# Kernel optimization log

Hardware: AMD Instinct MI355X
Metric: run time of the kernel (lower is better)

## Reference

```python
import math
import jax, jax.numpy as jnp
import numpy as np

N, E, EA = 25000, 400000, 400000
DN, DE, H = 256, 128, 8
DHN, DHE = DN // H, DE // H
EPS = 1e-5


def _ln(x, g, b):
    m = x.mean(-1, keepdims=True)
    v = ((x - m) ** 2).mean(-1, keepdims=True)
    return (x - m) * jax.lax.rsqrt(v + EPS) * g + b


def _scatter_softmax(scores, index, n):
    # per-segment stable softmax (matches torch scatter_reduce amax + scatter_add)
    m = jnp.maximum(jax.ops.segment_max(scores, index, num_segments=n), -1e9)
    ex = jnp.exp(scores - m[index])
    den = jax.ops.segment_sum(ex, index, num_segments=n)
    return ex / (den[index] + 1e-10)


def setup_inputs() -> dict:
    key = jax.random.key(0)
    ks = iter(jax.random.split(key, 64))
    rn = lambda shape, s=0.02: jax.random.normal(next(ks), shape, jnp.float32) * s
    inp = {
        'node_features': jax.random.normal(next(ks), (N, DN), jnp.float32),
        'edge_features': jax.random.normal(next(ks), (E, DE), jnp.float32),
        'edge_index': jax.random.randint(next(ks), (2, E), 0, N),
        'edge_adj': jax.random.randint(next(ks), (2, EA), 0, E),
        # NodeAttention params
        'n_Wq': rn((DN, DN)), 'n_bq': jnp.zeros(DN), 'n_Wk': rn((DN, DN)), 'n_bk': jnp.zeros(DN),
        'n_Wv': rn((DN, DN)), 'n_bv': jnp.zeros(DN), 'n_Web': rn((DE, H)), 'n_beb': jnp.zeros(H),
        'n_Wo': rn((DN, DN)), 'n_bo': jnp.zeros(DN), 'n_logt': jnp.zeros(H),
        'n_g': jnp.ones(DN), 'n_b': jnp.zeros(DN),
        # EdgeAttention params
        'e_Wq': rn((DE, DE)), 'e_bq': jnp.zeros(DE), 'e_Wk': rn((DE, DE)), 'e_bk': jnp.zeros(DE),
        'e_Wv': rn((DE, DE)), 'e_bv': jnp.zeros(DE), 'e_Wctx': rn((2 * DN, H)), 'e_bctx': jnp.zeros(H),
        'e_Wo': rn((DE, DE)), 'e_bo': jnp.zeros(DE), 'e_logt': jnp.zeros(H),
        'e_g': jnp.ones(DE), 'e_b': jnp.zeros(DE),
        # ReconciliationBridge params
        'r_We': rn((DE + 2 * DN, DE)), 'r_be': jnp.zeros(DE), 'r_eg': jnp.ones(DE), 'r_ebt': jnp.zeros(DE),
        'r_Wn': rn((DN + DE, DN)), 'r_bn': jnp.zeros(DN), 'r_ng': jnp.ones(DN), 'r_nbt': jnp.zeros(DN),
    }
    return inp


def reference(node_features, edge_features, edge_index, edge_adj,
              n_Wq, n_bq, n_Wk, n_bk, n_Wv, n_bv, n_Web, n_beb, n_Wo, n_bo, n_logt, n_g, n_b,
              e_Wq, e_bq, e_Wk, e_bk, e_Wv, e_bv, e_Wctx, e_bctx, e_Wo, e_bo, e_logt, e_g, e_b,
              r_We, r_be, r_eg, r_ebt, r_Wn, r_bn, r_ng, r_nbt):
    Nn, En = node_features.shape[0], edge_features.shape[0]
    src, tgt = edge_index[0], edge_index[1]

    # ---- NodeAttention (uses original node/edge features) ----
    x = node_features
    Q = (x @ n_Wq + n_bq).reshape(Nn, H, DHN)
    K = (x @ n_Wk + n_bk).reshape(Nn, H, DHN)
    V = (x @ n_Wv + n_bv).reshape(Nn, H, DHN)
    s = (Q[tgt] * K[src]).sum(-1) / math.sqrt(DHN)            # [E, H]
    s = (s + edge_features @ n_Web + n_beb) * jnp.exp(n_logt)
    w = _scatter_softmax(s, tgt, Nn)
    agg = jax.ops.segment_sum(V[src] * w[..., None], tgt, num_segments=Nn).reshape(Nn, DN)
    node_out = _ln(x + agg @ n_Wo + n_bo, n_g, n_b)

    # ---- EdgeAttention (uses original node/edge features) ----
    e = edge_features
    Qe = (e @ e_Wq + e_bq).reshape(En, H, DHE)
    Ke = (e @ e_Wk + e_bk).reshape(En, H, DHE)
    Ve = (e @ e_Wv + e_bv).reshape(En, H, DHE)
    se, te = edge_adj[0], edge_adj[1]
    s2 = (Qe[te] * Ke[se]).sum(-1) / math.sqrt(DHE)           # [EA, H]
    ctx = jnp.concatenate([node_features[src[se]], node_features[tgt[se]]], -1)
    s2 = (s2 + ctx @ e_Wctx + e_bctx) * jnp.exp(e_logt)
    w2 = _scatter_softmax(s2, te, En)
    agg2 = jax.ops.segment_sum(Ve[se] * w2[..., None], te, num_segments=En).reshape(En, DE)
    edge_out = _ln(e + agg2 @ e_Wo + e_bo, e_g, e_b)

    # ---- ReconciliationBridge on updated features ----
    edge_ctx = jnp.concatenate([edge_out, node_out[src], node_out[tgt]], -1)
    new_edges = _ln(edge_out + edge_ctx @ r_We + r_be, r_eg, r_ebt)
    all_nodes = jnp.concatenate([src, tgt])
    all_edges = jnp.concatenate([new_edges, new_edges], 0)
    esum = jax.ops.segment_sum(all_edges, all_nodes, num_segments=Nn)
    ecnt = jax.ops.segment_sum(jnp.ones(all_nodes.shape[0], jnp.float32), all_nodes, num_segments=Nn)
    emean = esum / (ecnt[:, None] + 1e-10)
    node_ctx = jnp.concatenate([node_out, emean], -1)
    new_nodes = _ln(node_out + node_ctx @ r_Wn + r_bn, r_ng, r_nbt)
    return new_nodes, new_edges
```

## Files before the change

kernel.cpp:

```cpp
#include <hip/hip_runtime.h>
#include <cstdio>
#include <cstddef>

typedef unsigned short u16;
typedef unsigned int u32;

#define DEVFN __device__ __forceinline__

namespace {
constexpr int NN = 25000;
constexpr int NE = 400000;
constexpr int NA = 400000;
constexpr int DN = 256;
constexpr int DE = 128;
constexpr int H  = 8;
constexpr float LN_EPS = 1e-5f;
}

DEVFN float bf2f(u32 x) { union { u32 u; float f; } v; v.u = x << 16; return v.f; }
DEVFN u16 f2bf(float f) {
    u32 u = __float_as_uint(f);
    u32 r = 0x7fffu + ((u >> 16) & 1u);
    return (u16)((u + r) >> 16);
}
DEVFN void unpack8(uint4 v, float* f) {
    f[0] = bf2f(v.x & 0xffffu); f[1] = bf2f(v.x >> 16);
    f[2] = bf2f(v.y & 0xffffu); f[3] = bf2f(v.y >> 16);
    f[4] = bf2f(v.z & 0xffffu); f[5] = bf2f(v.z >> 16);
    f[6] = bf2f(v.w & 0xffffu); f[7] = bf2f(v.w >> 16);
}

typedef __bf16 bf16x8 __attribute__((ext_vector_type(8)));
typedef float f32x4 __attribute__((ext_vector_type(4)));
union B8 { uint4 u; bf16x8 b; };

template<int B> struct IO;
template<> struct IO<1> {
    static DEVFN float ld(const void* p, size_t i) { return bf2f(((const u16*)p)[i]); }
    static DEVFN void ld8(const void* p, size_t i, float* f) {
        unpack8(*reinterpret_cast<const uint4*>((const u16*)p + i), f);
    }
    static DEVFN void st(void* p, size_t i, float v) { ((u16*)p)[i] = f2bf(v); }
};
template<> struct IO<0> {
    static DEVFN float ld(const void* p, size_t i) { return ((const float*)p)[i]; }
    static DEVFN void ld8(const void* p, size_t i, float* f) {
        const float* q = (const float*)p + i;
        float4 a = *reinterpret_cast<const float4*>(q);
        float4 b = *reinterpret_cast<const float4*>(q + 4);
        f[0]=a.x; f[1]=a.y; f[2]=a.z; f[3]=a.w; f[4]=b.x; f[5]=b.y; f[6]=b.z; f[7]=b.w;
    }
    static DEVFN void st(void* p, size_t i, float v) { ((float*)p)[i] = v; }
};

__global__ void k_detect(const void* ng, int* flag) {
    if (threadIdx.x == 0 && blockIdx.x == 0) {
        const u16* p = (const u16*)ng;
        int zeros = 0;
        for (int i = 0; i < 64; i += 2) if (p[i] == 0) ++zeros;
        *flag = (zeros >= 16) ? 0 : 1;
    }
}

__global__ __launch_bounds__(256) void k_fill(float* p, long n, float v) {
    long i = (long)blockIdx.x * 256 + threadIdx.x;
    long st = (long)gridDim.x * 256;
    for (; i < n; i += st) p[i] = v;
}

__global__ __launch_bounds__(256) void k_transpose(
    const int* dflag, const u16* __restrict__ in, u16* __restrict__ out, int K, int Nd)
{
    if (*dflag != 1) return;
    int gid = blockIdx.x * 256 + threadIdx.x;
    if (gid >= K * Nd) return;
    int n = gid / K, k = gid - n * K;
    out[gid] = in[(size_t)k * Nd + n];
}

__global__ __launch_bounds__(256) void k_gemm_mfma(
    const int* dflag, const u16* __restrict__ A, const u16* __restrict__ Wt,
    const u16* __restrict__ bias, u16* __restrict__ out, int M, int K, int Nd)
{
    if (*dflag != 1) return;
    __shared__ __align__(16) char shbuf[128 * 128];
    const int t = threadIdx.x;
    const int m0 = blockIdx.x * 64;
    const int n0 = blockIdx.y * 128;
    const int w = t >> 6;
    const int lane = t & 63;
    const int lm = lane & 15, lg = lane >> 4;
    const int NC = K >> 6;

    uint4 sreg[4];
    auto gstage = [&](int kc) {
#pragma unroll
        for (int it = 0; it < 4; ++it) {
            int idx = it * 256 + t;
            int n = idx >> 3, slot = idx & 7;
            sreg[it] = *reinterpret_cast<const uint4*>(Wt + (size_t)(n0 + n) * K + kc * 64 + slot * 8);
        }
    };
    auto swrite = [&]() {
#pragma unroll
        for (int it = 0; it < 4; ++it) {
            int idx = it * 256 + t;
            int n = idx >> 3, slot = idx & 7;
            *reinterpret_cast<uint4*>(shbuf + n * 128 + ((slot ^ (n & 7)) * 16)) = sreg[it];
        }
    };

    f32x4 acc[4][2];
    const f32x4 z = {0.f, 0.f, 0.f, 0.f};
#pragma unroll
    for (int mf = 0; mf < 4; ++mf)
#pragma unroll
        for (int nf = 0; nf < 2; ++nf) acc[mf][nf] = z;

    gstage(0); swrite();
    for (int kc = 0; kc < NC; ++kc) {
        if (kc + 1 < NC) gstage(kc + 1);
        __syncthreads();
#pragma unroll
        for (int ksl = 0; ksl < 2; ++ksl) {
            B8 a[4];
#pragma unroll
            for (int mf = 0; mf < 4; ++mf) {
                int r = m0 + mf * 16 + lm;
                if (r >= M) r = M - 1;
                a[mf].u = *reinterpret_cast<const uint4*>(A + (size_t)r * K + kc * 64 + ksl * 32 + lg * 8);
            }
#pragma unroll
            for (int nf = 0; nf < 2; ++nf) {
                int n = w * 32 + nf * 16 + lm;
                int slot = ksl * 4 + lg;
                B8 bfrag;
                bfrag.u = *reinterpret_cast<const uint4*>(shbuf + n * 128 + ((slot ^ (n & 7)) * 16));
#pragma unroll
                for (int mf = 0; mf < 4; ++mf)
                    acc[mf][nf] = __builtin_amdgcn_mfma_f32_16x16x32_bf16(a[mf].b, bfrag.b, acc[mf][nf], 0, 0, 0);
            }
        }
        __syncthreads();
        if (kc + 1 < NC) swrite();
    }
#pragma unroll
    for (int mf = 0; mf < 4; ++mf)
#pragma unroll
        for (int nf = 0; nf < 2; ++nf) {
            int col = n0 + w * 32 + nf * 16 + lm;
            float bb = bf2f(bias[col]);
#pragma unroll
            for (int j = 0; j < 4; ++j) {
                int gr = m0 + mf * 16 + lg * 4 + j;
                if (gr < M) out[(size_t)gr * Nd + col] = f2bf(acc[mf][nf][j] + bb);
            }
        }
}

template<int B>
__global__ __launch_bounds__(256) void k_edge_bias(
    const int* dflag, const void* __restrict__ ef, const void* __restrict__ Web,
    const void* __restrict__ beb, float* __restrict__ s)
{
    if (*dflag != B) return;
    __shared__ float Wsh[DE * H];
    __shared__ float bsh[H];
    for (int i = threadIdx.x; i < DE * H; i += 256) Wsh[i] = IO<B>::ld(Web, i);
    if (threadIdx.x < H) bsh[threadIdx.x] = IO<B>::ld(beb, threadIdx.x);
    __syncthreads();
    int gid = blockIdx.x * 256 + threadIdx.x;
    if (gid >= NE * H) return;
    int e = gid >> 3, h = gid & 7;
    float acc = 0.f;
    for (int k = 0; k < DE; k += 8) {
        float a[8]; IO<B>::ld8(ef, (size_t)e * DE + k, a);
#pragma unroll
        for (int j = 0; j < 8; ++j) acc += a[j] * Wsh[(k + j) * H + h];
    }
    s[gid] = acc + bsh[h];
}

template<int B>
__global__ __launch_bounds__(256) void k_ctx_bias(
    const int* dflag, const void* __restrict__ nf,
    const int* __restrict__ src, const int* __restrict__ tgt,
    const void* __restrict__ Wctx, const void* __restrict__ bctx, float* __restrict__ ebias)
{
    if (*dflag != B) return;
    __shared__ float Wsh[2 * DN * H];
    __shared__ float bsh[H];
    for (int i = threadIdx.x; i < 2 * DN * H; i += 256) Wsh[i] = IO<B>::ld(Wctx, i);
    if (threadIdx.x < H) bsh[threadIdx.x] = IO<B>::ld(bctx, threadIdx.x);
    __syncthreads();
    int gid = blockIdx.x * 256 + threadIdx.x;
    if (gid >= NE * H) return;
    int e = gid >> 3, h = gid & 7;
    int is = src[e], it = tgt[e];
    if ((unsigned)is >= NN || (unsigned)it >= NN) { ebias[gid] = 0.f; return; }
    float acc = 0.f;
    for (int k = 0; k < DN; k += 8) {
        float a[8]; IO<B>::ld8(nf, (size_t)is * DN + k, a);
#pragma unroll
        for (int j = 0; j < 8; ++j) acc += a[j] * Wsh[(k + j) * H + h];
    }
    for (int k = 0; k < DN; k += 8) {
        float a[8]; IO<B>::ld8(nf, (size_t)it * DN + k, a);
#pragma unroll
        for (int j = 0; j < 8; ++j) acc += a[j] * Wsh[(DN + k + j) * H + h];
    }
    ebias[gid] = acc + bsh[h];
}

template<int B>
__global__ __launch_bounds__(256) void k_node_score(
    const int* dflag, const u16* __restrict__ Q, const u16* __restrict__ Kt,
    const int* __restrict__ src, const int* __restrict__ tgt,
    const void* __restrict__ logt, float* __restrict__ s, float* __restrict__ den)
{
    if (*dflag != B) return;
    int gid = blockIdx.x * 256 + threadIdx.x;
    if (gid >= NE * H) return;
    int e = gid >> 3, h = gid & 7;
    int te = tgt[e], se = src[e];
    if ((unsigned)te >= NN || (unsigned)se >= NN) { s[gid] = 0.f; return; }
    const u16* q = Q + (size_t)te * DN + h * 32;
    const u16* k = Kt + (size_t)se * DN + h * 32;
    float acc = 0.f;
#pragma unroll
    for (int i = 0; i < 4; ++i) {
        float qa[8], ka[8];
        unpack8(*reinterpret_cast<const uint4*>(q + i * 8), qa);
        unpack8(*reinterpret_cast<const uint4*>(k + i * 8), ka);
#pragma unroll
        for (int j = 0; j < 8; ++j) acc += qa[j] * ka[j];
    }
    float val = (acc * 0.17677669529663689f + s[gid]) * expf(IO<B>::ld(logt, h));
    float ex = expf(fminf(val, 60.f));
    s[gid] = ex;
    atomicAdd(&den[(size_t)te * H + h], ex);
}

__global__ __launch_bounds__(256) void k_node_agg(
    const u16* __restrict__ V, const int* __restrict__ src, const int* __restrict__ tgt,
    const float* __restrict__ s, const float* __restrict__ den, float* __restrict__ agg)
{
    long gid = (long)blockIdx.x * 256 + threadIdx.x;
    if (gid >= (long)NE * DN) return;
    int e = (int)(gid >> 8);
    int c = (int)(gid & 255);
    int h = c >> 5;
    int te = tgt[e], se = src[e];
    if ((unsigned)te >= NN || (unsigned)se >= NN) return;
    float w = s[(size_t)e * H + h] / (den[(size_t)te * H + h] + 1e-10f);
    float v = bf2f(V[(size_t)se * DN + c]);
    atomicAdd(&agg[(size_t)te * DN + c], v * w);
}

template<int B>
__global__ __launch_bounds__(256) void k_edge_score(
    const int* dflag, const u16* __restrict__ Qe, const u16* __restrict__ Ke,
    const int* __restrict__ se, const int* __restrict__ te,
    const void* __restrict__ logt, const float* __restrict__ ebias,
    float* __restrict__ s2, float* __restrict__ den2)
{
    if (*dflag != B) return;
    int gid = blockIdx.x * 256 + threadIdx.x;
    if (gid >= NA * H) return;
    int a = gid >> 3, h = gid & 7;
    int tE = te[a], sE = se[a];
    if ((unsigned)tE >= NE || (unsigned)sE >= NE) { s2[gid] = 0.f; return; }
    const u16* q = Qe + (size_t)tE * DE + h * 16;
    const u16* k = Ke + (size_t)sE * DE + h * 16;
    float acc = 0.f;
#pragma unroll
    for (int i = 0; i < 2; ++i) {
        float qa[8], ka[8];
        unpack8(*reinterpret_cast<const uint4*>(q + i * 8), qa);
        unpack8(*reinterpret_cast<const uint4*>(k + i * 8), ka);
#pragma unroll
        for (int j = 0; j < 8; ++j) acc += qa[j] * ka[j];
    }
    float val = (acc * 0.25f + ebias[(size_t)sE * H + h]) * expf(IO<B>::ld(logt, h));
    float ex = expf(fminf(val, 60.f));
    s2[gid] = ex;
    atomicAdd(&den2[(size_t)tE * H + h], ex);
}

__global__ __launch_bounds__(256) void k_edge_agg(
    const u16* __restrict__ Ve, const int* __restrict__ se, const int* __restrict__ te,
    const float* __restrict__ s2, const float* __restrict__ den2, float* __restrict__ agg2)
{
    long gid = (long)blockIdx.x * 256 + threadIdx.x;
    if (gid >= (long)NA * DE) return;
    int a = (int)(gid >> 7);
    int c = (int)(gid & 127);
    int h = c >> 4;
    int tE = te[a], sE = se[a];
    if ((unsigned)tE >= NE || (unsigned)sE >= NE) return;
    float w = s2[(size_t)a * H + h] / (den2[(size_t)tE * H + h] + 1e-10f);
    float v = bf2f(Ve[(size_t)sE * DE + c]);
    atomicAdd(&agg2[(size_t)tE * DE + c], v * w);
}

template<int B>
__global__ __launch_bounds__(256) void k_node_out(
    const int* dflag, const float* __restrict__ agg, const void* __restrict__ x,
    const void* __restrict__ Wo, const void* __restrict__ bo,
    const void* __restrict__ g, const void* __restrict__ b, u16* __restrict__ nout)
{
    if (*dflag != B) return;
    __shared__ __align__(16) float As[32][36];
    __shared__ __align__(16) float Ws[32][264];
    const int t = threadIdx.x;
    const int m0 = blockIdx.x * 32;
    const int r0 = (t >> 5) * 4;
    const int c0 = (t & 31) * 8;
    const int arow = t >> 3, akk = (t & 7) * 4;
    const int wrow = t >> 3, wcc = (t & 7) * 32;
    float acc[4][8] = {};
    for (int k0 = 0; k0 < DN; k0 += 32) {
        float av[4];
        const int gr = m0 + arow;
        if (gr < NN) {
            float4 v = *reinterpret_cast<const float4*>(agg + (size_t)gr * DN + k0 + akk);
            av[0] = v.x; av[1] = v.y; av[2] = v.z; av[3] = v.w;
        } else { av[0] = av[1] = av[2] = av[3] = 0.f; }
        float wv[32];
#pragma unroll
        for (int u = 0; u < 4; ++u)
            IO<B>::ld8(Wo, (size_t)(k0 + wrow) * DN + wcc + u * 8, wv + u * 8);
        __syncthreads();
#pragma unroll
        for (int j = 0; j < 4; ++j) As[akk + j][arow] = av[j];
#pragma unroll
        for (int j = 0; j < 32; ++j) Ws[wrow][wcc + j] = wv[j];
        __syncthreads();
#pragma unroll
        for (int kk = 0; kk < 32; ++kk) {
            float4 a4 = *reinterpret_cast<const float4*>(&As[kk][r0]);
            float4 wa = *reinterpret_cast<const float4*>(&Ws[kk][c0]);
            float4 wb = *reinterpret_cast<const float4*>(&Ws[kk][c0 + 4]);
            float aa[4] = {a4.x, a4.y, a4.z, a4.w};
            float ww[8] = {wa.x, wa.y, wa.z, wa.w, wb.x, wb.y, wb.z, wb.w};
#pragma unroll
            for (int i = 0; i < 4; ++i)
#pragma unroll
                for (int j = 0; j < 8; ++j) acc[i][j] += aa[i] * ww[j];
        }
        __syncthreads();
    }
    float gv[8], bv[8], bov[8];
#pragma unroll
    for (int j = 0; j < 8; ++j) {
        gv[j] = IO<B>::ld(g, c0 + j); bv[j] = IO<B>::ld(b, c0 + j); bov[j] = IO<B>::ld(bo, c0 + j);
    }
#pragma unroll
    for (int i = 0; i < 4; ++i) {
        int gr = m0 + r0 + i;
        if (gr >= NN) continue;
        float xv[8]; IO<B>::ld8(x, (size_t)gr * DN + c0, xv);
        float val[8]; float sum = 0.f, sq = 0.f;
#pragma unroll
        for (int j = 0; j < 8; ++j) {
            val[j] = acc[i][j] + xv[j] + bov[j];
            sum += val[j]; sq += val[j] * val[j];
        }
#pragma unroll
        for (int msk = 1; msk < 32; msk <<= 1) {
            sum += __shfl_xor(sum, msk, 64);
            sq += __shfl_xor(sq, msk, 64);
        }
        float mu = sum * (1.f / DN);
        float var = fmaxf(sq * (1.f / DN) - mu * mu, 0.f);
        float rstd = rsqrtf(var + LN_EPS);
        u16* o = nout + (size_t)gr * DN + c0;
#pragma unroll
        for (int j = 0; j < 8; ++j) o[j] = f2bf((val[j] - mu) * rstd * gv[j] + bv[j]);
    }
}

template<int B>
__global__ __launch_bounds__(256) void k_edge_out(
    const int* dflag, const float* __restrict__ agg2, const void* __restrict__ ef,
    const void* __restrict__ Wo, const void* __restrict__ bo,
    const void* __restrict__ g, const void* __restrict__ b, u16* __restrict__ eout)
{
    if (*dflag != B) return;
    __shared__ __align__(16) float As[32][68];
    __shared__ __align__(16) float Ws[32][136];
    const int t = threadIdx.x;
    const int m0 = blockIdx.x * 64;
    const int r0 = (t >> 4) * 4;
    const int c0 = (t & 15) * 8;
    const int arow = t >> 2, akk = (t & 3) * 8;
    const int wrow = t >> 3, wcc = (t & 7) * 16;
    float acc[4][8] = {};
    for (int k0 = 0; k0 < DE; k0 += 32) {
        float av[8];
        {
            const float* p = agg2 + (size_t)(m0 + arow) * DE + k0 + akk;
            float4 v0 = *reinterpret_cast<const float4*>(p);
            float4 v1 = *reinterpret_cast<const float4*>(p + 4);
            av[0] = v0.x; av[1] = v0.y; av[2] = v0.z; av[3] = v0.w;
            av[4] = v1.x; av[5] = v1.y; av[6] = v1.z; av[7] = v1.w;
        }
        float wv[16];
        IO<B>::ld8(Wo, (size_t)(k0 + wrow) * DE + wcc, wv);
        IO<B>::ld8(Wo, (size_t)(k0 + wrow) * DE + wcc + 8, wv + 8);
        __syncthreads();
#pragma unroll
        for (int j = 0; j < 8; ++j) As[akk + j][arow] = av[j];
#pragma unroll
        for (int j = 0; j < 16; ++j) Ws[wrow][wcc + j] = wv[j];
        __syncthreads();
#pragma unroll
        for (int kk = 0; kk < 32; ++kk) {
            float4 a4 = *reinterpret_cast<const float4*>(&As[kk][r0]);
            float4 wa = *reinterpret_cast<const float4*>(&Ws[kk][c0]);
            float4 wb = *reinterpret_cast<const float4*>(&Ws[kk][c0 + 4]);
            float aa[4] = {a4.x, a4.y, a4.z, a4.w};
            float ww[8] = {wa.x, wa.y, wa.z, wa.w, wb.x, wb.y, wb.z, wb.w};
#pragma unroll
            for (int i = 0; i < 4; ++i)
#pragma unroll
                for (int j = 0; j < 8; ++j) acc[i][j] += aa[i] * ww[j];
        }
        __syncthreads();
    }
    float gv[8], bv[8], bov[8];
#pragma unroll
    for (int j = 0; j < 8; ++j) {
        gv[j] = IO<B>::ld(g, c0 + j); bv[j] = IO<B>::ld(b, c0 + j); bov[j] = IO<B>::ld(bo, c0 + j);
    }
#pragma unroll
    for (int i = 0; i < 4; ++i) {
        int gr = m0 + r0 + i;
        float xv[8]; IO<B>::ld8(ef, (size_t)gr * DE + c0, xv);
        float val[8]; float sum = 0.f, sq = 0.f;
#pragma unroll
        for (int j = 0; j < 8; ++j) {
            val[j] = acc[i][j] + xv[j] + bov[j];
            sum += val[j]; sq += val[j] * val[j];
        }
#pragma unroll
        for (int msk = 1; msk < 16; msk <<= 1) {
            sum += __shfl_xor(sum, msk, 64);
            sq += __shfl_xor(sq, msk, 64);
        }
        float mu = sum * (1.f / DE);
        float var = fmaxf(sq * (1.f / DE) - mu * mu, 0.f);
        float rstd = rsqrtf(var + LN_EPS);
        u16* o = eout + (size_t)gr * DE + c0;
#pragma unroll
        for (int j = 0; j < 8; ++j) o[j] = f2bf((val[j] - mu) * rstd * gv[j] + bv[j]);
    }
}

__global__ __launch_bounds__(256) void k_bridge_edge_mfma(
    const int* dflag, const u16* __restrict__ eout, const u16* __restrict__ nout,
    const int* __restrict__ src, const int* __restrict__ tgt,
    const u16* __restrict__ Wt, const u16* __restrict__ be,
    const u16* __restrict__ g, const u16* __restrict__ b,
    u16* __restrict__ out_edges)
{
    if (*dflag != 1) return;
    __shared__ __align__(16) char shbuf[64 * 132 * 4];
    __shared__ int es_sh[64], et_sh[64];
    const int t = threadIdx.x;
    const int m0 = blockIdx.x * 64;
    if (t < 64) {
        int a = src[m0 + t], c = tgt[m0 + t];
        es_sh[t] = ((unsigned)a < NN) ? a : 0;
        et_sh[t] = ((unsigned)c < NN) ? c : 0;
    }
    const int w = t >> 6;
    const int lane = t & 63;
    const int lm = lane & 15, lg = lane >> 4;
    constexpr int K = 640, NC = 10;

    uint4 sreg[4];
    auto gstage = [&](int kc) {
#pragma unroll
        for (int it = 0; it < 4; ++it) {
            int idx = it * 256 + t;
            int n = idx >> 3, slot = idx & 7;
            sreg[it] = *reinterpret_cast<const uint4*>(Wt + (size_t)n * K + kc * 64 + slot * 8);
        }
    };
    auto swrite = [&]() {
#pragma unroll
        for (int it = 0; it < 4; ++it) {
            int idx = it * 256 + t;
            int n = idx >> 3, slot = idx & 7;
            *reinterpret_cast<uint4*>(shbuf + n * 128 + ((slot ^ (n & 7)) * 16)) = sreg[it];
        }
    };

    f32x4 acc[4][2];
    const f32x4 z = {0.f, 0.f, 0.f, 0.f};
#pragma unroll
    for (int mf = 0; mf < 4; ++mf)
#pragma unroll
        for (int nf = 0; nf < 2; ++nf) acc[mf][nf] = z;

    gstage(0); swrite();
    for (int kc = 0; kc < NC; ++kc) {
        if (kc + 1 < NC) gstage(kc + 1);
        __syncthreads();
#pragma unroll
        for (int ksl = 0; ksl < 2; ++ksl) {
            B8 a[4];
#pragma unroll
            for (int mf = 0; mf < 4; ++mf) {
                int rloc = mf * 16 + lm;
                const u16* ap;
                if (kc < 2)      ap = eout + (size_t)(m0 + rloc) * DE + kc * 64;
                else if (kc < 6) ap = nout + (size_t)es_sh[rloc] * DN + (kc - 2) * 64;
                else             ap = nout + (size_t)et_sh[rloc] * DN + (kc - 6) * 64;
                a[mf].u = *reinterpret_cast<const uint4*>(ap + ksl * 32 + lg * 8);
            }
#pragma unroll
            for (int nf = 0; nf < 2; ++nf) {
                int n = w * 32 + nf * 16 + lm;
                int slot = ksl * 4 + lg;
                B8 bfrag;
                bfrag.u = *reinterpret_cast<const uint4*>(shbuf + n * 128 + ((slot ^ (n & 7)) * 16));
#pragma unroll
                for (int mf = 0; mf < 4; ++mf)
                    acc[mf][nf] = __builtin_amdgcn_mfma_f32_16x16x32_bf16(a[mf].b, bfrag.b, acc[mf][nf], 0, 0, 0);
            }
        }
        __syncthreads();
        if (kc + 1 < NC) swrite();
    }
    float* cex = (float*)shbuf;
#pragma unroll
    for (int mf = 0; mf < 4; ++mf)
#pragma unroll
        for (int nf = 0; nf < 2; ++nf)
#pragma unroll
            for (int j = 0; j < 4; ++j)
                cex[(mf * 16 + lg * 4 + j) * 132 + (w * 32 + nf * 16 + lm)] = acc[mf][nf][j];
    __syncthreads();
    {
        const int row = t >> 2, seg = t & 3;
        const int gr = m0 + row;
        const int cb = seg * 32;
        float v[32]; float sum = 0.f, sq = 0.f;
#pragma unroll
        for (int u = 0; u < 4; ++u) {
            float ev[8], bev[8];
            unpack8(*reinterpret_cast<const uint4*>(eout + (size_t)gr * DE + cb + u * 8), ev);
            unpack8(*reinterpret_cast<const uint4*>(be + cb + u * 8), bev);
#pragma unroll
            for (int j = 0; j < 8; ++j) {
                float x = cex[row * 132 + cb + u * 8 + j] + ev[j] + bev[j];
                v[u * 8 + j] = x; sum += x; sq += x * x;
            }
        }
        sum += __shfl_xor(sum, 1, 64); sq += __shfl_xor(sq, 1, 64);
        sum += __shfl_xor(sum, 2, 64); sq += __shfl_xor(sq, 2, 64);
        float mu = sum * (1.f / DE);
        float rstd = rsqrtf(fmaxf(sq * (1.f / DE) - mu * mu, 0.f) + LN_EPS);
#pragma unroll
        for (int u = 0; u < 4; ++u) {
            float gv[8], bv[8];
            unpack8(*reinterpret_cast<const uint4*>(g + cb + u * 8), gv);
            unpack8(*reinterpret_cast<const uint4*>(b + cb + u * 8), bv);
#pragma unroll
            for (int j = 0; j < 8; ++j)
                out_edges[(size_t)gr * DE + cb + u * 8 + j] = f2bf((v[u * 8 + j] - mu) * rstd * gv[j] + bv[j]);
        }
    }
}

template<int B>
__global__ __launch_bounds__(256) void k_gemm_bias(
    const int* dflag, const void* __restrict__ A, const void* __restrict__ W,
    const void* __restrict__ bias, u16* __restrict__ out, int M, int K, int Nd)
{
    if (*dflag != B) return;
    __shared__ __align__(16) float As[32][72];
    __shared__ __align__(16) float Ws[32][68];
    const int t = threadIdx.x;
    const int m0 = blockIdx.x * 64;
    const int n0 = blockIdx.y * 64;
    const int r0 = (t >> 4) * 4;
    const int c0 = (t & 15) * 4;
    const int arow = t >> 2, akk = (t & 3) * 8;
    const int wrow = t >> 3, wcc = (t & 7) * 8;
    float acc[4][4] = {};
    for (int k0 = 0; k0 < K; k0 += 32) {
        float av[8];
        const int gr = m0 + arow;
        if (gr < M) IO<B>::ld8(A, (size_t)gr * K + k0 + akk, av);
        else { for (int j = 0; j < 8; ++j) av[j] = 0.f; }
        float wv[8];
        IO<B>::ld8(W, (size_t)(k0 + wrow) * Nd + n0 + wcc, wv);
        __syncthreads();
#pragma unroll
        for (int j = 0; j < 8; ++j) As[akk + j][arow] = av[j];
#pragma unroll
        for (int j = 0; j < 8; ++j) Ws[wrow][wcc + j] = wv[j];
        __syncthreads();
#pragma unroll
        for (int kk = 0; kk < 32; ++kk) {
            float4 a4 = *reinterpret_cast<const float4*>(&As[kk][r0]);
            float4 w4 = *reinterpret_cast<const float4*>(&Ws[kk][c0]);
            float aa[4] = {a4.x, a4.y, a4.z, a4.w};
            float ww[4] = {w4.x, w4.y, w4.z, w4.w};
#pragma unroll
            for (int i = 0; i < 4; ++i)
#pragma unroll
                for (int j = 0; j < 4; ++j) acc[i][j] += aa[i] * ww[j];
        }
        __syncthreads();
    }
    float bv[4];
#pragma unroll
    for (int j = 0; j < 4; ++j) bv[j] = IO<B>::ld(bias, n0 + c0 + j);
#pragma unroll
    for (int i = 0; i < 4; ++i) {
        int gr = m0 + r0 + i;
        if (gr < M) {
            u16* o = out + (size_t)gr * Nd + n0 + c0;
#pragma unroll
            for (int j = 0; j < 4; ++j) o[j] = f2bf(acc[i][j] + bv[j]);
        }
    }
}

template<int B>
__global__ __launch_bounds__(256) void k_bridge_edge(
    const int* dflag, const u16* __restrict__ eout, const u16* __restrict__ nout,
    const int* __restrict__ src, const int* __restrict__ tgt,
    const void* __restrict__ We, const void* __restrict__ be,
    const void* __restrict__ g, const void* __restrict__ b,
    void* __restrict__ out_edges)
{
    if (*dflag != B) return;
    __shared__ __align__(16) float As[32][68];
    __shared__ __align__(16) float Ws[32][136];
    __shared__ int es[64], et[64];
    const int t = threadIdx.x;
    const int m0 = blockIdx.x * 64;
    if (t < 64) {
        int a = src[m0 + t], c = tgt[m0 + t];
        es[t] = ((unsigned)a < NN) ? a : 0;
        et[t] = ((unsigned)c < NN) ? c : 0;
    }
    __syncthreads();
    const int r0 = (t >> 4) * 4;
    const int c0 = (t & 15) * 8;
    const int arow = t >> 2, akk = (t & 3) * 8;
    const int wrow = t >> 3, wcc = (t & 7) * 16;
    float acc[4][8] = {};
    for (int k0 = 0; k0 < 640; k0 += 32) {
        const u16* aptr;
        if (k0 < 128)      aptr = eout + (size_t)(m0 + arow) * DE + k0 + akk;
        else if (k0 < 384) aptr = nout + (size_t)es[arow] * DN + (k0 - 128) + akk;
        else               aptr = nout + (size_t)et[arow] * DN + (k0 - 384) + akk;
        float av[8]; unpack8(*reinterpret_cast<const uint4*>(aptr), av);
        float wv[16];
        IO<B>::ld8(We, (size_t)(k0 + wrow) * DE + wcc, wv);
        IO<B>::ld8(We, (size_t)(k0 + wrow) * DE + wcc + 8, wv + 8);
        __syncthreads();
#pragma unroll
        for (int j = 0; j < 8; ++j) As[akk + j][arow] = av[j];
#pragma unroll
        for (int j = 0; j < 16; ++j) Ws[wrow][wcc + j] = wv[j];
        __syncthreads();
#pragma unroll
        for (int kk = 0; kk < 32; ++kk) {
            float4 a4 = *reinterpret_cast<const float4*>(&As[kk][r0]);
            float4 wa = *reinterpret_cast<const float4*>(&Ws[kk][c0]);
            float4 wb = *reinterpret_cast<const float4*>(&Ws[kk][c0 + 4]);
            float aa[4] = {a4.x, a4.y, a4.z, a4.w};
            float ww[8] = {wa.x, wa.y, wa.z, wa.w, wb.x, wb.y, wb.z, wb.w};
#pragma unroll
            for (int i = 0; i < 4; ++i)
#pragma unroll
                for (int j = 0; j < 8; ++j) acc[i][j] += aa[i] * ww[j];
        }
        __syncthreads();
    }
    float gv[8], bv[8], bev[8];
#pragma unroll
    for (int j = 0; j < 8; ++j) {
        gv[j] = IO<B>::ld(g, c0 + j); bv[j] = IO<B>::ld(b, c0 + j); bev[j] = IO<B>::ld(be, c0 + j);
    }
#pragma unroll
    for (int i = 0; i < 4; ++i) {
        int r = r0 + i;
        int gr = m0 + r;
        float val[8]; float sum = 0.f, sq = 0.f;
#pragma unroll
        for (int j = 0; j < 8; ++j) {
            val[j] = acc[i][j] + bf2f(eout[(size_t)gr * DE + c0 + j]) + bev[j];
            sum += val[j]; sq += val[j] * val[j];
        }
#pragma unroll
        for (int msk = 1; msk < 16; msk <<= 1) {
            sum += __shfl_xor(sum, msk, 64);
            sq += __shfl_xor(sq, msk, 64);
        }
        float mu = sum * (1.f / DE);
        float var = fmaxf(sq * (1.f / DE) - mu * mu, 0.f);
        float rstd = rsqrtf(var + LN_EPS);
#pragma unroll
        for (int j = 0; j < 8; ++j) {
            float ov = (val[j] - mu) * rstd * gv[j] + bv[j];
            IO<B>::st(out_edges, (size_t)gr * DE + c0 + j, ov);
        }
    }
}

__global__ __launch_bounds__(256) void k_deg(
    const int* __restrict__ src, const int* __restrict__ tgt, int* __restrict__ cnt)
{
    int e = blockIdx.x * 256 + threadIdx.x;
    if (e >= NE) return;
    int a = src[e]; a = ((unsigned)a < NN) ? a : 0;
    int c = tgt[e]; c = ((unsigned)c < NN) ? c : 0;
    atomicAdd(&cnt[a], 1);
    atomicAdd(&cnt[c], 1);
}

__global__ __launch_bounds__(256) void k_scan(
    const int* __restrict__ cnt, int* __restrict__ off, int* __restrict__ cur, int n)
{
    __shared__ int sh[256];
    __shared__ int carry;
    const int t = threadIdx.x;
    if (t == 0) carry = 0;
    __syncthreads();
    for (int base = 0; base < n; base += 256) {
        int i = base + t;
        int v = (i < n) ? cnt[i] : 0;
        sh[t] = v;
        __syncthreads();
#pragma unroll
        for (int d = 1; d < 256; d <<= 1) {
            int x = (t >= d) ? sh[t - d] : 0;
            __syncthreads();
            sh[t] += x;
            __syncthreads();
        }
        int incl = sh[t];
        int total = sh[255];
        if (i < n) {
            off[i + 1] = carry + incl;
            cur[i] = carry + incl - v;
        }
        __syncthreads();
        if (t == 0) carry += total;
        __syncthreads();
    }
    if (t == 0) off[0] = 0;
}

__global__ __launch_bounds__(256) void k_place(
    const int* __restrict__ src, const int* __restrict__ tgt,
    int* __restrict__ cur, int* __restrict__ ent)
{
    int e = blockIdx.x * 256 + threadIdx.x;
    if (e >= NE) return;
    int a = src[e]; a = ((unsigned)a < NN) ? a : 0;
    int c = tgt[e]; c = ((unsigned)c < NN) ? c : 0;
    int p = atomicAdd(&cur[a], 1); ent[p] = e;
    p = atomicAdd(&cur[c], 1);     ent[p] = e;
}

template<int B>
__global__ __launch_bounds__(256) void k_esum_gather(
    const int* dflag, const void* __restrict__ edges ,
    const int* __restrict__ off, const int* __restrict__ ent,
    float* __restrict__ esum, float* __restrict__ ecnt)
{
    if (*dflag != B) return;
    int node = blockIdx.x * 4 + (threadIdx.x >> 6);
    if (node >= NN) return;
    int lane = threadIdx.x & 63;
    int b0 = off[node], b1 = off[node + 1];
    float a0 = 0.f, a1 = 0.f;
    for (int i = b0; i < b1; ++i) {
        int e = ent[i];
        size_t base = (size_t)e * DE;
        a0 += IO<B>::ld(edges, base + lane);
        a1 += IO<B>::ld(edges, base + 64 + lane);
    }
    esum[(size_t)node * DE + lane] = a0;
    esum[(size_t)node * DE + 64 + lane] = a1;
    if (lane == 0) ecnt[node] = (float)(b1 - b0);
}

template<int B>
__global__ __launch_bounds__(256) void k_bridge_node(
    const int* dflag, const u16* __restrict__ nout,
    const float* __restrict__ esum, const float* __restrict__ ecnt,
    const void* __restrict__ Wn, const void* __restrict__ bn,
    const void* __restrict__ g, const void* __restrict__ b, void* __restrict__ out_nodes)
{
    if (*dflag != B) return;
    __shared__ __align__(16) float As[32][36];
    __shared__ __align__(16) float Ws[32][264];
    __shared__ float rc[32];
    const int t = threadIdx.x;
    const int m0 = blockIdx.x * 32;
    if (t < 32) {
        int gr = m0 + t;
        rc[t] = (gr < NN) ? 1.f / (ecnt[gr] + 1e-10f) : 0.f;
    }
    __syncthreads();
    const int r0 = (t >> 5) * 4;
    const int c0 = (t & 31) * 8;
    const int arow = t >> 3, akk = (t & 7) * 4;
    const int wrow = t >> 3, wcc = (t & 7) * 32;
    float acc[4][8] = {};
    for (int k0 = 0; k0 < 384; k0 += 32) {
        float av[4];
        const int gr = m0 + arow;
        if (gr < NN) {
            if (k0 < 256) {
                uint2 v = *reinterpret_cast<const uint2*>(nout + (size_t)gr * DN + k0 + akk);
                av[0] = bf2f(v.x & 0xffffu); av[1] = bf2f(v.x >> 16);
                av[2] = bf2f(v.y & 0xffffu); av[3] = bf2f(v.y >> 16);
            } else {
                float4 v = *reinterpret_cast<const float4*>(esum + (size_t)gr * DE + (k0 - 256) + akk);
                float r = rc[arow];
                av[0] = v.x * r; av[1] = v.y * r; av[2] = v.z * r; av[3] = v.w * r;
            }
        } else { av[0] = av[1] = av[2] = av[3] = 0.f; }
        float wv[32];
#pragma unroll
        for (int u = 0; u < 4; ++u)
            IO<B>::ld8(Wn, (size_t)(k0 + wrow) * DN + wcc + u * 8, wv + u * 8);
        __syncthreads();
#pragma unroll
        for (int j = 0; j < 4; ++j) As[akk + j][arow] = av[j];
#pragma unroll
        for (int j = 0; j < 32; ++j) Ws[wrow][wcc + j] = wv[j];
        __syncthreads();
#pragma unroll
        for (int kk = 0; kk < 32; ++kk) {
            float4 a4 = *reinterpret_cast<const float4*>(&As[kk][r0]);
            float4 wa = *reinterpret_cast<const float4*>(&Ws[kk][c0]);
            float4 wb = *reinterpret_cast<const float4*>(&Ws[kk][c0 + 4]);
            float aa[4] = {a4.x, a4.y, a4.z, a4.w};
            float ww[8] = {wa.x, wa.y, wa.z, wa.w, wb.x, wb.y, wb.z, wb.w};
#pragma unroll
            for (int i = 0; i < 4; ++i)
#pragma unroll
                for (int j = 0; j < 8; ++j) acc[i][j] += aa[i] * ww[j];
        }
        __syncthreads();
    }
    float gv[8], bv[8], bnv[8];
#pragma unroll
    for (int j = 0; j < 8; ++j) {
        gv[j] = IO<B>::ld(g, c0 + j); bv[j] = IO<B>::ld(b, c0 + j); bnv[j] = IO<B>::ld(bn, c0 + j);
    }
#pragma unroll
    for (int i = 0; i < 4; ++i) {
        int gr = m0 + r0 + i;
        if (gr >= NN) continue;
        float val[8]; float sum = 0.f, sq = 0.f;
#pragma unroll
        for (int j = 0; j < 8; ++j) {
            val[j] = acc[i][j] + bf2f(nout[(size_t)gr * DN + c0 + j]) + bnv[j];
            sum += val[j]; sq += val[j] * val[j];
        }
#pragma unroll
        for (int msk = 1; msk < 32; msk <<= 1) {
            sum += __shfl_xor(sum, msk, 64);
            sq += __shfl_xor(sq, msk, 64);
        }
        float mu = sum * (1.f / DN);
        float var = fmaxf(sq * (1.f / DN) - mu * mu, 0.f);
        float rstd = rsqrtf(var + LN_EPS);
#pragma unroll
        for (int j = 0; j < 8; ++j)
            IO<B>::st(out_nodes, (size_t)gr * DN + c0 + j, (val[j] - mu) * rstd * gv[j] + bv[j]);
    }
}

extern "C" void kernel_launch(void* const* d_in, const int* in_sizes, int n_in,
                              void* d_out, int out_size, void* d_ws, size_t ws_size,
                              hipStream_t stream)
{
    if (n_in < 38 || in_sizes[0] != NN * DN || in_sizes[1] != NE * DE) {
        fprintf(stderr, "kernel_launch: unexpected inputs n_in=%d sz0=%d sz1=%d\n",
                n_in, in_sizes[0], n_in > 1 ? in_sizes[1] : -1);
        return;
    }
    const void* nf  = d_in[0];
    const void* ef  = d_in[1];
    const int* eidx = (const int*)d_in[2];
    const int* eadj = (const int*)d_in[3];
    const int* srcN = eidx;
    const int* tgtN = eidx + NE;
    const int* seA  = eadj;
    const int* teA  = eadj + NA;
    const void *nWq = d_in[4],  *nbq  = d_in[5];
    const void *nWk = d_in[6],  *nbk  = d_in[7];
    const void *nWv = d_in[8],  *nbv  = d_in[9];
    const void *nWeb = d_in[10], *nbeb = d_in[11];
    const void *nWo = d_in[12], *nbo  = d_in[13];
    const void *nlogt = d_in[14], *ng = d_in[15], *nb = d_in[16];
    const void *eWq = d_in[17], *ebq  = d_in[18];
    const void *eWk = d_in[19], *ebk  = d_in[20];
    const void *eWv = d_in[21], *ebv  = d_in[22];
    const void *eWctx = d_in[23], *ebctx = d_in[24];
    const void *eWo = d_in[25], *ebo  = d_in[26];
    const void *elogt = d_in[27], *eg = d_in[28], *ebb = d_in[29];
    const void *rWe = d_in[30], *rbe  = d_in[31];
    const void *reg_ = d_in[32], *rebt = d_in[33];
    const void *rWn = d_in[34], *rbn  = d_in[35];
    const void *rng = d_in[36], *rnbt = d_in[37];

    char* ws = (char*)d_ws;
    size_t off = 0;
    auto take = [&](size_t bytes) -> char* {
        char* p = ws + off;
        off = (off + bytes + 255) & ~(size_t)255;
        return p;
    };
    int*   flag     = (int*)  take(256);
    u16*   node_out = (u16*)  take((size_t)NN * DN * 2);
    u16*   edge_out = (u16*)  take((size_t)NE * DE * 2);
    float* esum     = (float*)take((size_t)NN * DE * 4);
    float* ecnt     = (float*)take((size_t)NN * 4);
    u16* WtQn = (u16*)take((size_t)DN * DN * 2);
    u16* WtKn = (u16*)take((size_t)DN * DN * 2);
    u16* WtVn = (u16*)take((size_t)DN * DN * 2);
    u16* WtQe = (u16*)take((size_t)DE * DE * 2);
    u16* WtKe = (u16*)take((size_t)DE * DE * 2);
    u16* WtVe = (u16*)take((size_t)DE * DE * 2);
    u16* WtWe = (u16*)take((size_t)640 * DE * 2);
    const size_t T = off;
    u16*   Qn   = (u16*)(ws + T);
    u16*   Kn   = Qn + (size_t)NN * DN;
    u16*   Vn   = Kn + (size_t)NN * DN;
    float* sA   = (float*)(Vn + (size_t)NN * DN);
    float* denA = sA + (size_t)NE * H;
    float* aggA = denA + (size_t)NN * H;
    size_t endA = (size_t)((char*)(aggA + (size_t)NN * DN) - ws);
    u16*   Qe    = (u16*)(ws + T);
    u16*   Ke    = Qe + (size_t)NE * DE;
    float* agg2  = (float*)Ke;
    float* ebias = (float*)(ws + T + (size_t)NE * DE * 2 + (size_t)NE * DE * 4);
    float* s2    = ebias + (size_t)NE * H;
    float* den2  = s2 + (size_t)NA * H;
    size_t endB = (size_t)((char*)(den2 + (size_t)NE * H) - ws);
    int* c_off = (int*)(ws + T);
    int* c_cur = c_off + (NN + 1);
    int* c_ent = c_cur + NN;
    size_t endC = (size_t)((char*)(c_ent + (size_t)2 * NE) - ws);
    size_t need = endA > endB ? endA : endB;
    if (endC > need) need = endC;
    if (ws_size < need) {
        fprintf(stderr, "kernel_launch: ws_size=%zu < needed=%zu\n", ws_size, need);
        return;
    }

    auto fill = [&](float* p, long n, float v) {
        long blocks = (n + 255) / 256;
        if (blocks > 8192) blocks = 8192;
        k_fill<<<dim3((unsigned)blocks), dim3(256), 0, stream>>>(p, n, v);
    };

    k_detect<<<1, 64, 0, stream>>>(ng, flag);

    auto T2D = [&](const void* W, u16* Wt, int K, int Nd) {
        k_transpose<<<dim3((unsigned)((K * Nd + 255) / 256)), 256, 0, stream>>>(flag, (const u16*)W, Wt, K, Nd);
    };
    T2D(nWq, WtQn, DN, DN); T2D(nWk, WtKn, DN, DN); T2D(nWv, WtVn, DN, DN);
    T2D(eWq, WtQe, DE, DE); T2D(eWk, WtKe, DE, DE); T2D(eWv, WtVe, DE, DE);
    T2D(rWe, WtWe, 640, DE);

    fill(denA, (long)NN * H, 0.f);
    fill(aggA, (long)NN * DN, 0.f);
    dim3 gA((NN + 63) / 64, DN / 64);
    dim3 gAm((NN + 63) / 64, DN / 128);
    k_gemm_mfma<<<gAm, 256, 0, stream>>>(flag, (const u16*)nf, WtQn, (const u16*)nbq, Qn, NN, DN, DN);
    k_gemm_bias<0><<<gA, 256, 0, stream>>>(flag, nf, nWq, nbq, Qn, NN, DN, DN);
    k_gemm_mfma<<<gAm, 256, 0, stream>>>(flag, (const u16*)nf, WtKn, (const u16*)nbk, Kn, NN, DN, DN);
    k_gemm_bias<0><<<gA, 256, 0, stream>>>(flag, nf, nWk, nbk, Kn, NN, DN, DN);
    k_gemm_mfma<<<gAm, 256, 0, stream>>>(flag, (const u16*)nf, WtVn, (const u16*)nbv, Vn, NN, DN, DN);
    k_gemm_bias<0><<<gA, 256, 0, stream>>>(flag, nf, nWv, nbv, Vn, NN, DN, DN);
    const int gEH = (NE * H + 255) / 256;
    k_edge_bias<1><<<gEH, 256, 0, stream>>>(flag, ef, nWeb, nbeb, sA);
    k_edge_bias<0><<<gEH, 256, 0, stream>>>(flag, ef, nWeb, nbeb, sA);
    k_node_score<1><<<gEH, 256, 0, stream>>>(flag, Qn, Kn, srcN, tgtN, nlogt, sA, denA);
    k_node_score<0><<<gEH, 256, 0, stream>>>(flag, Qn, Kn, srcN, tgtN, nlogt, sA, denA);
    {
        long n = (long)NE * DN;
        k_node_agg<<<dim3((unsigned)((n + 255) / 256)), 256, 0, stream>>>(Vn, srcN, tgtN, sA, denA, aggA);
    }
    k_node_out<1><<<(NN + 31) / 32, 256, 0, stream>>>(flag, aggA, nf, nWo, nbo, ng, nb, node_out);
    k_node_out<0><<<(NN + 31) / 32, 256, 0, stream>>>(flag, aggA, nf, nWo, nbo, ng, nb, node_out);

    dim3 gB(NE / 64, DE / 64);
    dim3 gBm(NE / 64, DE / 128);
    k_gemm_mfma<<<gBm, 256, 0, stream>>>(flag, (const u16*)ef, WtQe, (const u16*)ebq, Qe, NE, DE, DE);
    k_gemm_bias<0><<<gB, 256, 0, stream>>>(flag, ef, eWq, ebq, Qe, NE, DE, DE);
    k_gemm_mfma<<<gBm, 256, 0, stream>>>(flag, (const u16*)ef, WtKe, (const u16*)ebk, Ke, NE, DE, DE);
    k_gemm_bias<0><<<gB, 256, 0, stream>>>(flag, ef, eWk, ebk, Ke, NE, DE, DE);
    k_ctx_bias<1><<<gEH, 256, 0, stream>>>(flag, nf, srcN, tgtN, eWctx, ebctx, ebias);
    k_ctx_bias<0><<<gEH, 256, 0, stream>>>(flag, nf, srcN, tgtN, eWctx, ebctx, ebias);
    fill(den2, (long)NE * H, 0.f);
    const int gAH = (NA * H + 255) / 256;
    k_edge_score<1><<<gAH, 256, 0, stream>>>(flag, Qe, Ke, seA, teA, elogt, ebias, s2, den2);
    k_edge_score<0><<<gAH, 256, 0, stream>>>(flag, Qe, Ke, seA, teA, elogt, ebias, s2, den2);
    k_gemm_mfma<<<gBm, 256, 0, stream>>>(flag, (const u16*)ef, WtVe, (const u16*)ebv, Qe , NE, DE, DE);
    k_gemm_bias<0><<<gB, 256, 0, stream>>>(flag, ef, eWv, ebv, Qe , NE, DE, DE);
    fill(agg2, (long)NE * DE, 0.f);
    {
        long n = (long)NA * DE;
        k_edge_agg<<<dim3((unsigned)((n + 255) / 256)), 256, 0, stream>>>(Qe , seA, teA, s2, den2, agg2);
    }
    k_edge_out<1><<<NE / 64, 256, 0, stream>>>(flag, agg2, ef, eWo, ebo, eg, ebb, edge_out);
    k_edge_out<0><<<NE / 64, 256, 0, stream>>>(flag, agg2, ef, eWo, ebo, eg, ebb, edge_out);

    void* out_nodes = d_out;
    void* out_edges_bf = (void*)((u16*)d_out + (size_t)NN * DN);
    void* out_edges_f  = (void*)((float*)d_out + (size_t)NN * DN);
    k_bridge_edge_mfma<<<NE / 64, 256, 0, stream>>>(flag, edge_out, node_out, srcN, tgtN,
                                                    WtWe, (const u16*)rbe, (const u16*)reg_, (const u16*)rebt,
                                                    (u16*)out_edges_bf);
    k_bridge_edge<0><<<NE / 64, 256, 0, stream>>>(flag, edge_out, node_out, srcN, tgtN,
                                                  rWe, rbe, reg_, rebt, out_edges_f);
    fill((float*)c_cur, NN, 0.f);
    k_deg<<<(NE + 255) / 256, 256, 0, stream>>>(srcN, tgtN, c_cur);
    k_scan<<<1, 256, 0, stream>>>(c_cur , c_off, c_cur , NN);
    k_place<<<(NE + 255) / 256, 256, 0, stream>>>(srcN, tgtN, c_cur, c_ent);
    k_esum_gather<1><<<(NN + 3) / 4, 256, 0, stream>>>(flag, out_edges_bf, c_off, c_ent, esum, ecnt);
    k_esum_gather<0><<<(NN + 3) / 4, 256, 0, stream>>>(flag, out_edges_f, c_off, c_ent, esum, ecnt);
    k_bridge_node<1><<<(NN + 31) / 32, 256, 0, stream>>>(flag, node_out, esum, ecnt,
                                                         rWn, rbn, rng, rnbt, out_nodes);
    k_bridge_node<0><<<(NN + 31) / 32, 256, 0, stream>>>(flag, node_out, esum, ecnt,
                                                         rWn, rbn, rng, rnbt, out_nodes);
}
```

Measured before the change: 3.770 ms.

## Move output projections and bridge node GEMM to MFMA, unify fp32/bf16 paths

Replaces the scalar FP32 shared-memory GEMMs in node_out, edge_out and bridge_node with bf16 MFMA tiles. Their weights are pre-transposed and converted once per call, and the accumulators are staged through LDS for the fused residual+LayerNorm epilogue. The MFMA GEMM is templated so the fp32 input path also uses MFMA by packing activations to bf16 on load. This cuts FP32 ALU time on the dense projections, at the cost of bf16 rounding of agg and activations and extra transpose launches.

```diff
diff --git a/kernel.cpp b/kernel.cpp
--- a/kernel.cpp
+++ b/kernel.cpp
@@ -33,6 +33,8 @@
 typedef __bf16 bf16x8 __attribute__((ext_vector_type(8)));
 typedef float f32x4 __attribute__((ext_vector_type(4)));
 union B8 { uint4 u; bf16x8 b; };
+
+DEVFN u32 pk2(float a, float b) { return (u32)f2bf(a) | ((u32)f2bf(b) << 16); }
 
 template<int B> struct IO;
 template<> struct IO<1> {
@@ -53,6 +55,36 @@
     static DEVFN void st(void* p, size_t i, float v) { ((float*)p)[i] = v; }
 };
 
+template<int B> DEVFN B8 ldA8(const void* A, size_t off) {
+    B8 r;
+    if constexpr (B == 1) {
+        r.u = *reinterpret_cast<const uint4*>((const u16*)A + off);
+    } else {
+        const float* p = (const float*)A + off;
+        float4 x = *reinterpret_cast<const float4*>(p);
+        float4 y = *reinterpret_cast<const float4*>(p + 4);
+        r.u.x = pk2(x.x, x.y); r.u.y = pk2(x.z, x.w);
+        r.u.z = pk2(y.x, y.y); r.u.w = pk2(y.z, y.w);
+    }
+    return r;
+}
+DEVFN B8 ldF8(const float* p) {
+    float4 x = *reinterpret_cast<const float4*>(p);
+    float4 y = *reinterpret_cast<const float4*>(p + 4);
+    B8 r;
+    r.u.x = pk2(x.x, x.y); r.u.y = pk2(x.z, x.w);
+    r.u.z = pk2(y.x, y.y); r.u.w = pk2(y.z, y.w);
+    return r;
+}
+DEVFN B8 ldF8s(const float* p, float s) {
+    float4 x = *reinterpret_cast<const float4*>(p);
+    float4 y = *reinterpret_cast<const float4*>(p + 4);
+    B8 r;
+    r.u.x = pk2(x.x*s, x.y*s); r.u.y = pk2(x.z*s, x.w*s);
+    r.u.z = pk2(y.x*s, y.y*s); r.u.w = pk2(y.z*s, y.w*s);
+    return r;
+}
+
 __global__ void k_detect(const void* ng, int* flag) {
     if (threadIdx.x == 0 && blockIdx.x == 0) {
         const u16* p = (const u16*)ng;
@@ -68,21 +100,23 @@
     for (; i < n; i += st) p[i] = v;
 }
 
-__global__ __launch_bounds__(256) void k_transpose(
-    const int* dflag, const u16* __restrict__ in, u16* __restrict__ out, int K, int Nd)
-{
-    if (*dflag != 1) return;
+template<int B>
+__global__ __launch_bounds__(256) void k_transpose_cvt(
+    const int* dflag, const void* __restrict__ in, u16* __restrict__ out, int K, int Nd)
+{
+    if (*dflag != B) return;
     int gid = blockIdx.x * 256 + threadIdx.x;
     if (gid >= K * Nd) return;
     int n = gid / K, k = gid - n * K;
-    out[gid] = in[(size_t)k * Nd + n];
-}
-
+    out[gid] = f2bf(IO<B>::ld(in, (size_t)k * Nd + n));
+}
+
+template<int B>
 __global__ __launch_bounds__(256) void k_gemm_mfma(
-    const int* dflag, const u16* __restrict__ A, const u16* __restrict__ Wt,
-    const u16* __restrict__ bias, u16* __restrict__ out, int M, int K, int Nd)
-{
-    if (*dflag != 1) return;
+    const int* dflag, const void* __restrict__ A, const u16* __restrict__ Wt,
+    const void* __restrict__ bias, u16* __restrict__ out, int M, int K, int Nd)
+{
+    if (*dflag != B) return;
     __shared__ __align__(16) char shbuf[128 * 128];
     const int t = threadIdx.x;
     const int m0 = blockIdx.x * 64;
@@ -128,7 +162,7 @@
             for (int mf = 0; mf < 4; ++mf) {
                 int r = m0 + mf * 16 + lm;
                 if (r >= M) r = M - 1;
-                a[mf].u = *reinterpret_cast<const uint4*>(A + (size_t)r * K + kc * 64 + ksl * 32 + lg * 8);
+                a[mf] = ldA8<B>(A, (size_t)r * K + kc * 64 + ksl * 32 + lg * 8);
             }
 #pragma unroll
             for (int nf = 0; nf < 2; ++nf) {
@@ -149,7 +183,7 @@
 #pragma unroll
         for (int nf = 0; nf < 2; ++nf) {
             int col = n0 + w * 32 + nf * 16 + lm;
-            float bb = bf2f(bias[col]);
+            float bb = IO<B>::ld(bias, col);
 #pragma unroll
             for (int j = 0; j < 4; ++j) {
                 int gr = m0 + mf * 16 + lg * 4 + j;
@@ -304,167 +338,222 @@
 }
 
 template<int B>
-__global__ __launch_bounds__(256) void k_node_out(
+__global__ __launch_bounds__(256) void k_node_out_mfma(
     const int* dflag, const float* __restrict__ agg, const void* __restrict__ x,
-    const void* __restrict__ Wo, const void* __restrict__ bo,
+    const u16* __restrict__ Wt, const void* __restrict__ bo,
     const void* __restrict__ g, const void* __restrict__ b, u16* __restrict__ nout)
 {
     if (*dflag != B) return;
-    __shared__ __align__(16) float As[32][36];
-    __shared__ __align__(16) float Ws[32][264];
+    __shared__ __align__(16) char shbuf[32 * 264 * 4];
     const int t = threadIdx.x;
     const int m0 = blockIdx.x * 32;
-    const int r0 = (t >> 5) * 4;
-    const int c0 = (t & 31) * 8;
-    const int arow = t >> 3, akk = (t & 7) * 4;
-    const int wrow = t >> 3, wcc = (t & 7) * 32;
-    float acc[4][8] = {};
-    for (int k0 = 0; k0 < DN; k0 += 32) {
-        float av[4];
-        const int gr = m0 + arow;
+    const int w = t >> 6, lane = t & 63, lm = lane & 15, lg = lane >> 4;
+    constexpr int K = 256, NC = 4;
+
+    uint4 sreg[8];
+    auto gstage = [&](int kc) {
+#pragma unroll
+        for (int it = 0; it < 8; ++it) {
+            int idx = it * 256 + t;
+            int n = idx >> 3, slot = idx & 7;
+            sreg[it] = *reinterpret_cast<const uint4*>(Wt + (size_t)n * K + kc * 64 + slot * 8);
+        }
+    };
+    auto swrite = [&]() {
+#pragma unroll
+        for (int it = 0; it < 8; ++it) {
+            int idx = it * 256 + t;
+            int n = idx >> 3, slot = idx & 7;
+            *reinterpret_cast<uint4*>(shbuf + n * 128 + ((slot ^ (n & 7)) * 16)) = sreg[it];
+        }
+    };
+
+    f32x4 acc[2][4];
+    const f32x4 z = {0.f, 0.f, 0.f, 0.f};
+#pragma unroll
+    for (int mf = 0; mf < 2; ++mf)
+#pragma unroll
+        for (int nf = 0; nf < 4; ++nf) acc[mf][nf] = z;
+
+    gstage(0); swrite();
+    for (int kc = 0; kc < NC; ++kc) {
+        if (kc + 1 < NC) gstage(kc + 1);
+        __syncthreads();
+#pragma unroll
+        for (int ksl = 0; ksl < 2; ++ksl) {
+            B8 a[2];
+#pragma unroll
+            for (int mf = 0; mf < 2; ++mf) {
+                int r = m0 + mf * 16 + lm;
+                if (r >= NN) r = NN - 1;
+                a[mf] = ldF8(agg + (size_t)r * DN + kc * 64 + ksl * 32 + lg * 8);
+            }
+#pragma unroll
+            for (int nf = 0; nf < 4; ++nf) {
+                int n = w * 64 + nf * 16 + lm;
+                int slot = ksl * 4 + lg;
+                B8 bfrag;
+                bfrag.u = *reinterpret_cast<const uint4*>(shbuf + n * 128 + ((slot ^ (n & 7)) * 16));
+#pragma unroll
+                for (int mf = 0; mf < 2; ++mf)
+                    acc[mf][nf] = __builtin_amdgcn_mfma_f32_16x16x32_bf16(a[mf].b, bfrag.b, acc[mf][nf], 0, 0, 0);
+            }
+        }
+        __syncthreads();
+        if (kc + 1 < NC) swrite();
+    }
+    float* cex = (float*)shbuf;
+#pragma unroll
+    for (int mf = 0; mf < 2; ++mf)
+#pragma unroll
+        for (int nf = 0; nf < 4; ++nf)
+#pragma unroll
+            for (int j = 0; j < 4; ++j)
+                cex[(mf * 16 + lg * 4 + j) * 264 + (w * 64 + nf * 16 + lm)] = acc[mf][nf][j];
+    __syncthreads();
+    {
+        const int row = t >> 3, seg = t & 7;
+        const int gr = m0 + row;
         if (gr < NN) {
-            float4 v = *reinterpret_cast<const float4*>(agg + (size_t)gr * DN + k0 + akk);
-            av[0] = v.x; av[1] = v.y; av[2] = v.z; av[3] = v.w;
-        } else { av[0] = av[1] = av[2] = av[3] = 0.f; }
-        float wv[32];
-#pragma unroll
-        for (int u = 0; u < 4; ++u)
-            IO<B>::ld8(Wo, (size_t)(k0 + wrow) * DN + wcc + u * 8, wv + u * 8);
-        __syncthreads();
-#pragma unroll
-        for (int j = 0; j < 4; ++j) As[akk + j][arow] = av[j];
-#pragma unroll
-        for (int j = 0; j < 32; ++j) Ws[wrow][wcc + j] = wv[j];
-        __syncthreads();
-#pragma unroll
-        for (int kk = 0; kk < 32; ++kk) {
-            float4 a4 = *reinterpret_cast<const float4*>(&As[kk][r0]);
-            float4 wa = *reinterpret_cast<const float4*>(&Ws[kk][c0]);
-            float4 wb = *reinterpret_cast<const float4*>(&Ws[kk][c0 + 4]);
-            float aa[4] = {a4.x, a4.y, a4.z, a4.w};
-            float ww[8] = {wa.x, wa.y, wa.z, wa.w, wb.x, wb.y, wb.z, wb.w};
-#pragma unroll
-            for (int i = 0; i < 4; ++i)
-#pragma unroll
-                for (int j = 0; j < 8; ++j) acc[i][j] += aa[i] * ww[j];
-        }
-        __syncthreads();
-    }
-    float gv[8], bv[8], bov[8];
-#pragma unroll
-    for (int j = 0; j < 8; ++j) {
-        gv[j] = IO<B>::ld(g, c0 + j); bv[j] = IO<B>::ld(b, c0 + j); bov[j] = IO<B>::ld(bo, c0 + j);
-    }
-#pragma unroll
-    for (int i = 0; i < 4; ++i) {
-        int gr = m0 + r0 + i;
-        if (gr >= NN) continue;
-        float xv[8]; IO<B>::ld8(x, (size_t)gr * DN + c0, xv);
-        float val[8]; float sum = 0.f, sq = 0.f;
-#pragma unroll
-        for (int j = 0; j < 8; ++j) {
-            val[j] = acc[i][j] + xv[j] + bov[j];
-            sum += val[j]; sq += val[j] * val[j];
-        }
-#pragma unroll
-        for (int msk = 1; msk < 32; msk <<= 1) {
-            sum += __shfl_xor(sum, msk, 64);
-            sq += __shfl_xor(sq, msk, 64);
-        }
-        float mu = sum * (1.f / DN);
-        float var = fmaxf(sq * (1.f / DN) - mu * mu, 0.f);
-        float rstd = rsqrtf(var + LN_EPS);
-        u16* o = nout + (size_t)gr * DN + c0;
-#pragma unroll
-        for (int j = 0; j < 8; ++j) o[j] = f2bf((val[j] - mu) * rstd * gv[j] + bv[j]);
+            const int cb = seg * 32;
+            float v[32]; float sum = 0.f, sq = 0.f;
+#pragma unroll
+            for (int u = 0; u < 4; ++u) {
+                float xv[8]; IO<B>::ld8(x, (size_t)gr * DN + cb + u * 8, xv);
+#pragma unroll
+                for (int j = 0; j < 8; ++j) {
+                    float val = cex[row * 264 + cb + u * 8 + j] + xv[j] + IO<B>::ld(bo, cb + u * 8 + j);
+                    v[u * 8 + j] = val; sum += val; sq += val * val;
+                }
+            }
+            sum += __shfl_xor(sum, 1, 64); sq += __shfl_xor(sq, 1, 64);
+            sum += __shfl_xor(sum, 2, 64); sq += __shfl_xor(sq, 2, 64);
+            sum += __shfl_xor(sum, 4, 64); sq += __shfl_xor(sq, 4, 64);
+            float mu = sum * (1.f / DN);
+            float rstd = rsqrtf(fmaxf(sq * (1.f / DN) - mu * mu, 0.f) + LN_EPS);
+#pragma unroll
+            for (int u = 0; u < 4; ++u)
+#pragma unroll
+                for (int j = 0; j < 8; ++j) {
+                    int c = cb + u * 8 + j;
+                    nout[(size_t)gr * DN + c] =
+                        f2bf((v[u * 8 + j] - mu) * rstd * IO<B>::ld(g, c) + IO<B>::ld(b, c));
+                }
+        }
     }
 }
 
 template<int B>
-__global__ __launch_bounds__(256) void k_edge_out(
+__global__ __launch_bounds__(256) void k_edge_out_mfma(
     const int* dflag, const float* __restrict__ agg2, const void* __restrict__ ef,
-    const void* __restrict__ Wo, const void* __restrict__ bo,
+    const u16* __restrict__ Wt, const void* __restrict__ bo,
     const void* __restrict__ g, const void* __restrict__ b, u16* __restrict__ eout)
 {
     if (*dflag != B) return;
-    __shared__ __align__(16) float As[32][68];
-    __shared__ __align__(16) float Ws[32][136];
+    __shared__ __align__(16) char shbuf[64 * 132 * 4];
     const int t = threadIdx.x;
     const int m0 = blockIdx.x * 64;
-    const int r0 = (t >> 4) * 4;
-    const int c0 = (t & 15) * 8;
-    const int arow = t >> 2, akk = (t & 3) * 8;
-    const int wrow = t >> 3, wcc = (t & 7) * 16;
-    float acc[4][8] = {};
-    for (int k0 = 0; k0 < DE; k0 += 32) {
-        float av[8];
-        {
-            const float* p = agg2 + (size_t)(m0 + arow) * DE + k0 + akk;
-            float4 v0 = *reinterpret_cast<const float4*>(p);
-            float4 v1 = *reinterpret_cast<const float4*>(p + 4);
-            av[0] = v0.x; av[1] = v0.y; av[2] = v0.z; av[3] = v0.w;
-            av[4] = v1.x; av[5] = v1.y; av[6] = v1.z; av[7] = v1.w;
-        }
-        float wv[16];
-        IO<B>::ld8(Wo, (size_t)(k0 + wrow) * DE + wcc, wv);
-        IO<B>::ld8(Wo, (size_t)(k0 + wrow) * DE + wcc + 8, wv + 8);
-        __syncthreads();
-#pragma unroll
-        for (int j = 0; j < 8; ++j) As[akk + j][arow] = av[j];
-#pragma unroll
-        for (int j = 0; j < 16; ++j) Ws[wrow][wcc + j] = wv[j];
-        __syncthreads();
-#pragma unroll
-        for (int kk = 0; kk < 32; ++kk) {
-            float4 a4 = *reinterpret_cast<const float4*>(&As[kk][r0]);
-            float4 wa = *reinterpret_cast<const float4*>(&Ws[kk][c0]);
-            float4 wb = *reinterpret_cast<const float4*>(&Ws[kk][c0 + 4]);
-            float aa[4] = {a4.x, a4.y, a4.z, a4.w};
-            float ww[8] = {wa.x, wa.y, wa.z, wa.w, wb.x, wb.y, wb.z, wb.w};
-#pragma unroll
-            for (int i = 0; i < 4; ++i)
-#pragma unroll
-                for (int j = 0; j < 8; ++j) acc[i][j] += aa[i] * ww[j];
-        }
-        __syncthreads();
-    }
-    float gv[8], bv[8], bov[8];
-#pragma unroll
-    for (int j = 0; j < 8; ++j) {
-        gv[j] = IO<B>::ld(g, c0 + j); bv[j] = IO<B>::ld(b, c0 + j); bov[j] = IO<B>::ld(bo, c0 + j);
-    }
-#pragma unroll
-    for (int i = 0; i < 4; ++i) {
-        int gr = m0 + r0 + i;
-        float xv[8]; IO<B>::ld8(ef, (size_t)gr * DE + c0, xv);
-        float val[8]; float sum = 0.f, sq = 0.f;
-#pragma unroll
-        for (int j = 0; j < 8; ++j) {
-            val[j] = acc[i][j] + xv[j] + bov[j];
-            sum += val[j]; sq += val[j] * val[j];
-        }
-#pragma unroll
-        for (int msk = 1; msk < 16; msk <<= 1) {
-            sum += __shfl_xor(sum, msk, 64);
-            sq += __shfl_xor(sq, msk, 64);
-        }
+    const int w = t >> 6, lane = t & 63, lm = lane & 15, lg = lane >> 4;
+    constexpr int K = 128, NC = 2;
+
+    uint4 sreg[4];
+    auto gstage = [&](int kc) {
+#pragma unroll
+        for (int it = 0; it < 4; ++it) {
+            int idx = it * 256 + t;
+            int n = idx >> 3, slot = idx & 7;
+            sreg[it] = *reinterpret_cast<const uint4*>(Wt + (size_t)n * K + kc * 64 + slot * 8);
+        }
+    };
+    auto swrite = [&]() {
+#pragma unroll
+        for (int it = 0; it < 4; ++it) {
+            int idx = it * 256 + t;
+            int n = idx >> 3, slot = idx & 7;
+            *reinterpret_cast<uint4*>(shbuf + n * 128 + ((slot ^ (n & 7)) * 16)) = sreg[it];
+        }
+    };
+
+    f32x4 acc[4][2];
+    const f32x4 z = {0.f, 0.f, 0.f, 0.f};
+#pragma unroll
+    for (int mf = 0; mf < 4; ++mf)
+#pragma unroll
+        for (int nf = 0; nf < 2; ++nf) acc[mf][nf] = z;
+
+    gstage(0); swrite();
+    for (int kc = 0; kc < NC; ++kc) {
+        if (kc + 1 < NC) gstage(kc + 1);
+        __syncthreads();
+#pragma unroll
+        for (int ksl = 0; ksl < 2; ++ksl) {
+            B8 a[4];
+#pragma unroll
+            for (int mf = 0; mf < 4; ++mf) {
+                int r = m0 + mf * 16 + lm;
+                a[mf] = ldF8(agg2 + (size_t)r * DE + kc * 64 + ksl * 32 + lg * 8);
+            }
+#pragma unroll
+            for (int nf = 0; nf < 2; ++nf) {
+                int n = w * 32 + nf * 16 + lm;
+                int slot = ksl * 4 + lg;
+                B8 bfrag;
+                bfrag.u = *reinterpret_cast<const uint4*>(shbuf + n * 128 + ((slot ^ (n & 7)) * 16));
+#pragma unroll
+                for (int mf = 0; mf < 4; ++mf)
+                    acc[mf][nf] = __builtin_amdgcn_mfma_f32_16x16x32_bf16(a[mf].b, bfrag.b, acc[mf][nf], 0, 0, 0);
+            }
+        }
+        __syncthreads();
+        if (kc + 1 < NC) swrite();
+    }
+    float* cex = (float*)shbuf;
+#pragma unroll
+    for (int mf = 0; mf < 4; ++mf)
+#pragma unroll
+        for (int nf = 0; nf < 2; ++nf)
+#pragma unroll
+            for (int j = 0; j < 4; ++j)
+                cex[(mf * 16 + lg * 4 + j) * 132 + (w * 32 + nf * 16 + lm)] = acc[mf][nf][j];
+    __syncthreads();
+    {
+        const int row = t >> 2, seg = t & 3;
+        const int gr = m0 + row;
+        const int cb = seg * 32;
+        float v[32]; float sum = 0.f, sq = 0.f;
+#pragma unroll
+        for (int u = 0; u < 4; ++u) {
+            float xv[8]; IO<B>::ld8(ef, (size_t)gr * DE + cb + u * 8, xv);
+#pragma unroll
+            for (int j = 0; j < 8; ++j) {
+                float val = cex[row * 132 + cb + u * 8 + j] + xv[j] + IO<B>::ld(bo, cb + u * 8 + j);
+                v[u * 8 + j] = val; sum += val; sq += val * val;
+            }
+        }
+        sum += __shfl_xor(sum, 1, 64); sq += __shfl_xor(sq, 1, 64);
+        sum += __shfl_xor(sum, 2, 64); sq += __shfl_xor(sq, 2, 64);
         float mu = sum * (1.f / DE);
-        float var = fmaxf(sq * (1.f / DE) - mu * mu, 0.f);
-        float rstd = rsqrtf(var + LN_EPS);
-        u16* o = eout + (size_t)gr * DE + c0;
-#pragma unroll
-        for (int j = 0; j < 8; ++j) o[j] = f2bf((val[j] - mu) * rstd * gv[j] + bv[j]);
-    }
-}
-
+        float rstd = rsqrtf(fmaxf(sq * (1.f / DE) - mu * mu, 0.f) + LN_EPS);
+#pragma unroll
+        for (int u = 0; u < 4; ++u)
+#pragma unroll
+            for (int j = 0; j < 8; ++j) {
+                int c = cb + u * 8 + j;
+                eout[(size_t)gr * DE + c] =
+                    f2bf((v[u * 8 + j] - mu) * rstd * IO<B>::ld(g, c) + IO<B>::ld(b, c));
+            }
+    }
+}
+
+template<int B>
 __global__ __launch_bounds__(256) void k_bridge_edge_mfma(
     const int* dflag, const u16* __restrict__ eout, const u16* __restrict__ nout,
     const int* __restrict__ src, const int* __restrict__ tgt,
-    const u16* __restrict__ Wt, const u16* __restrict__ be,
-    const u16* __restrict__ g, const u16* __restrict__ b,
-    u16* __restrict__ out_edges)
-{
-    if (*dflag != 1) return;
+    const u16* __restrict__ Wt, const void* __restrict__ be,
+    const void* __restrict__ g, const void* __restrict__ b,
+    void* __restrict__ out_edges)
+{
+    if (*dflag != B) return;
     __shared__ __align__(16) char shbuf[64 * 132 * 4];
     __shared__ int es_sh[64], et_sh[64];
     const int t = threadIdx.x;
@@ -550,12 +639,11 @@
         float v[32]; float sum = 0.f, sq = 0.f;
 #pragma unroll
         for (int u = 0; u < 4; ++u) {
-            float ev[8], bev[8];
+            float ev[8];
             unpack8(*reinterpret_cast<const uint4*>(eout + (size_t)gr * DE + cb + u * 8), ev);
-            unpack8(*reinterpret_cast<const uint4*>(be + cb + u * 8), bev);
 #pragma unroll
             for (int j = 0; j < 8; ++j) {
-                float x = cex[row * 132 + cb + u * 8 + j] + ev[j] + bev[j];
+                float x = cex[row * 132 + cb + u * 8 + j] + ev[j] + IO<B>::ld(be, cb + u * 8 + j);
                 v[u * 8 + j] = x; sum += x; sq += x * x;
             }
         }
@@ -564,154 +652,128 @@
         float mu = sum * (1.f / DE);
         float rstd = rsqrtf(fmaxf(sq * (1.f / DE) - mu * mu, 0.f) + LN_EPS);
 #pragma unroll
-        for (int u = 0; u < 4; ++u) {
-            float gv[8], bv[8];
-            unpack8(*reinterpret_cast<const uint4*>(g + cb + u * 8), gv);
-            unpack8(*reinterpret_cast<const uint4*>(b + cb + u * 8), bv);
-#pragma unroll
-            for (int j = 0; j < 8; ++j)
-                out_edges[(size_t)gr * DE + cb + u * 8 + j] = f2bf((v[u * 8 + j] - mu) * rstd * gv[j] + bv[j]);
-        }
+        for (int u = 0; u < 4; ++u)
+#pragma unroll
+            for (int j = 0; j < 8; ++j) {
+                int c = cb + u * 8 + j;
+                IO<B>::st(out_edges, (size_t)gr * DE + c,
+                          (v[u * 8 + j] - mu) * rstd * IO<B>::ld(g, c) + IO<B>::ld(b, c));
+            }
     }
 }
 
 template<int B>
-__global__ __launch_bounds__(256) void k_gemm_bias(
-    const int* dflag, const void* __restrict__ A, const void* __restrict__ W,
-    const void* __restrict__ bias, u16* __restrict__ out, int M, int K, int Nd)
+__global__ __launch_bounds__(256) void k_bridge_node_mfma(
+    const int* dflag, const u16* __restrict__ nout,
+    const float* __restrict__ esum, const float* __restrict__ ecnt,
+    const u16* __restrict__ Wt, const void* __restrict__ bn,
+    const void* __restrict__ g, const void* __restrict__ b, void* __restrict__ out_nodes)
 {
     if (*dflag != B) return;
-    __shared__ __align__(16) float As[32][72];
-    __shared__ __align__(16) float Ws[32][68];
+    __shared__ __align__(16) char shbuf[32 * 264 * 4];
+    __shared__ float rc_sh[32];
     const int t = threadIdx.x;
-    const int m0 = blockIdx.x * 64;
-    const int n0 = blockIdx.y * 64;
-    const int r0 = (t >> 4) * 4;
-    const int c0 = (t & 15) * 4;
-    const int arow = t >> 2, akk = (t & 3) * 8;
-    const int wrow = t >> 3, wcc = (t & 7) * 8;
-    float acc[4][4] = {};
-    for (int k0 = 0; k0 < K; k0 += 32) {
-        float av[8];
-        const int gr = m0 + arow;
-        if (gr < M) IO<B>::ld8(A, (size_t)gr * K + k0 + akk, av);
-        else { for (int j = 0; j < 8; ++j) av[j] = 0.f; }
-        float wv[8];
-        IO<B>::ld8(W, (size_t)(k0 + wrow) * Nd + n0 + wcc, wv);
-        __syncthreads();
-#pragma unroll
-        for (int j = 0; j < 8; ++j) As[akk + j][arow] = av[j];
-#pragma unroll
-        for (int j = 0; j < 8; ++j) Ws[wrow][wcc + j] = wv[j];
-        __syncthreads();
-#pragma unroll
-        for (int kk = 0; kk < 32; ++kk) {
-            float4 a4 = *reinterpret_cast<const float4*>(&As[kk][r0]);
-            float4 w4 = *reinterpret_cast<const float4*>(&Ws[kk][c0]);
-            float aa[4] = {a4.x, a4.y, a4.z, a4.w};
-            float ww[4] = {w4.x, w4.y, w4.z, w4.w};
-#pragma unroll
-            for (int i = 0; i < 4; ++i)
-#pragma unroll
-                for (int j = 0; j < 4; ++j) acc[i][j] += aa[i] * ww[j];
-        }
-        __syncthreads();
-    }
-    float bv[4];
-#pragma unroll
-    for (int j = 0; j < 4; ++j) bv[j] = IO<B>::ld(bias, n0 + c0 + j);
-#pragma unroll
-    for (int i = 0; i < 4; ++i) {
-        int gr = m0 + r0 + i;
-        if (gr < M) {
-            u16* o = out + (size_t)gr * Nd + n0 + c0;
-#pragma unroll
-            for (int j = 0; j < 4; ++j) o[j] = f2bf(acc[i][j] + bv[j]);
-        }
-    }
-}
-
-template<int B>
-__global__ __launch_bounds__(256) void k_bridge_edge(
-    const int* dflag, const u16* __restrict__ eout, const u16* __restrict__ nout,
-    const int* __restrict__ src, const int* __restrict__ tgt,
-    const void* __restrict__ We, const void* __restrict__ be,
-    const void* __restrict__ g, const void* __restrict__ b,
-    void* __restrict__ out_edges)
-{
-    if (*dflag != B) return;
-    __shared__ __align__(16) float As[32][68];
-    __shared__ __align__(16) float Ws[32][136];
-    __shared__ int es[64], et[64];
-    const int t = threadIdx.x;
-    const int m0 = blockIdx.x * 64;
-    if (t < 64) {
-        int a = src[m0 + t], c = tgt[m0 + t];
-        es[t] = ((unsigned)a < NN) ? a : 0;
-        et[t] = ((unsigned)c < NN) ? c : 0;
-    }
+    const int m0 = blockIdx.x * 32;
+    if (t < 32) {
+        int gr = m0 + t;
+        rc_sh[t] = (gr < NN) ? 1.f / (ecnt[gr] + 1e-10f) : 0.f;
+    }
+    const int w = t >> 6, lane = t & 63, lm = lane & 15, lg = lane >> 4;
+    constexpr int K = 384, NC = 6;
+
+    uint4 sreg[8];
+    auto gstage = [&](int kc) {
+#pragma unroll
+        for (int it = 0; it < 8; ++it) {
+            int idx = it * 256 + t;
+            int n = idx >> 3, slot = idx & 7;
+            sreg[it] = *reinterpret_cast<const uint4*>(Wt + (size_t)n * K + kc * 64 + slot * 8);
+        }
+    };
+    auto swrite = [&]() {
+#pragma unroll
+        for (int it = 0; it < 8; ++it) {
+            int idx = it * 256 + t;
+            int n = idx >> 3, slot = idx & 7;
+            *reinterpret_cast<uint4*>(shbuf + n * 128 + ((slot ^ (n & 7)) * 16)) = sreg[it];
+        }
+    };
+
+    f32x4 acc[2][4];
+    const f32x4 z = {0.f, 0.f, 0.f, 0.f};
+#pragma unroll
+    for (int mf = 0; mf < 2; ++mf)
+#pragma unroll
+        for (int nf = 0; nf < 4; ++nf) acc[mf][nf] = z;
+
+    gstage(0); swrite();
+    for (int kc = 0; kc < NC; ++kc) {
+        if (kc + 1 < NC) gstage(kc + 1);
+        __syncthreads();
+#pragma unroll
+        for (int ksl = 0; ksl < 2; ++ksl) {
+            B8 a[2];
+#pragma unroll
+            for (int mf = 0; mf < 2; ++mf) {
+                int rl = mf * 16 + lm;
+                int r = m0 + rl; if (r >= NN) r = NN - 1;
+                if (kc < 4)
+                    a[mf].u = *reinterpret_cast<const uint4*>(nout + (size_t)r * DN + kc * 64 + ksl * 32 + lg * 8);
+                else
+                    a[mf] = ldF8s(esum + (size_t)r * DE + (kc - 4) * 64 + ksl * 32 + lg * 8, rc_sh[rl]);
+            }
+#pragma unroll
+            for (int nf = 0; nf < 4; ++nf) {
+                int n = w * 64 + nf * 16 + lm;
+                int slot = ksl * 4 + lg;
+                B8 bfrag;
+                bfrag.u = *reinterpret_cast<const uint4*>(shbuf + n * 128 + ((slot ^ (n & 7)) * 16));
+#pragma unroll
+                for (int mf = 0; mf < 2; ++mf)
+                    acc[mf][nf] = __builtin_amdgcn_mfma_f32_16x16x32_bf16(a[mf].b, bfrag.b, acc[mf][nf], 0, 0, 0);
+            }
+        }
+        __syncthreads();
+        if (kc + 1 < NC) swrite();
+    }
+    float* cex = (float*)shbuf;
+#pragma unroll
+    for (int mf = 0; mf < 2; ++mf)
+#pragma unroll
+        for (int nf = 0; nf < 4; ++nf)
+#pragma unroll
+            for (int j = 0; j < 4; ++j)
+                cex[(mf * 16 + lg * 4 + j) * 264 + (w * 64 + nf * 16 + lm)] = acc[mf][nf][j];
     __syncthreads();
-    const int r0 = (t >> 4) * 4;
-    const int c0 = (t & 15) * 8;
-    const int arow = t >> 2, akk = (t & 3) * 8;
-    const int wrow = t >> 3, wcc = (t & 7) * 16;
-    float acc[4][8] = {};
-    for (int k0 = 0; k0 < 640; k0 += 32) {
-        const u16* aptr;
-        if (k0 < 128)      aptr = eout + (size_t)(m0 + arow) * DE + k0 + akk;
-        else if (k0 < 384) aptr = nout + (size_t)es[arow] * DN + (k0 - 128) + akk;
-        else               aptr = nout + (size_t)et[arow] * DN + (k0 - 384) + akk;
-        float av[8]; unpack8(*reinterpret_cast<const uint4*>(aptr), av);
-        float wv[16];
-        IO<B>::ld8(We, (size_t)(k0 + wrow) * DE + wcc, wv);
-        IO<B>::ld8(We, (size_t)(k0 + wrow) * DE + wcc + 8, wv + 8);
-        __syncthreads();
-#pragma unroll
-        for (int j = 0; j < 8; ++j) As[akk + j][arow] = av[j];
-#pragma unroll
-        for (int j = 0; j < 16; ++j) Ws[wrow][wcc + j] = wv[j];
-        __syncthreads();
-#pragma unroll
-        for (int kk = 0; kk < 32; ++kk) {
-            float4 a4 = *reinterpret_cast<const float4*>(&As[kk][r0]);
-            float4 wa = *reinterpret_cast<const float4*>(&Ws[kk][c0]);
-            float4 wb = *reinterpret_cast<const float4*>(&Ws[kk][c0 + 4]);
-            float aa[4] = {a4.x, a4.y, a4.z, a4.w};
-            float ww[8] = {wa.x, wa.y, wa.z, wa.w, wb.x, wb.y, wb.z, wb.w};
-#pragma unroll
-            for (int i = 0; i < 4; ++i)
-#pragma unroll
-                for (int j = 0; j < 8; ++j) acc[i][j] += aa[i] * ww[j];
-        }
-        __syncthreads();
-    }
-    float gv[8], bv[8], bev[8];
-#pragma unroll
-    for (int j = 0; j < 8; ++j) {
-        gv[j] = IO<B>::ld(g, c0 + j); bv[j] = IO<B>::ld(b, c0 + j); bev[j] = IO<B>::ld(be, c0 + j);
-    }
-#pragma unroll
-    for (int i = 0; i < 4; ++i) {
-        int r = r0 + i;
-        int gr = m0 + r;
-        float val[8]; float sum = 0.f, sq = 0.f;
-#pragma unroll
-        for (int j = 0; j < 8; ++j) {
-            val[j] = acc[i][j] + bf2f(eout[(size_t)gr * DE + c0 + j]) + bev[j];
-            sum += val[j]; sq += val[j] * val[j];
-        }
-#pragma unroll
-        for (int msk = 1; msk < 16; msk <<= 1) {
-            sum += __shfl_xor(sum, msk, 64);
-            sq += __shfl_xor(sq, msk, 64);
-        }
-        float mu = sum * (1.f / DE);
-        float var = fmaxf(sq * (1.f / DE) - mu * mu, 0.f);
-        float rstd = rsqrtf(var + LN_EPS);
-#pragma unroll
-        for (int j = 0; j < 8; ++j) {
-            float ov = (val[j] - mu) * rstd * gv[j] + bv[j];
-            IO<B>::st(out_edges, (size_t)gr * DE + c0 + j, ov);
+    {
+        const int row = t >> 3, seg = t & 7;
+        const int gr = m0 + row;
+        if (gr < NN) {
+            const int cb = seg * 32;
+            float v[32]; float sum = 0.f, sq = 0.f;
+#pragma unroll
+            for (int u = 0; u < 4; ++u) {
+                float xv[8];
+                unpack8(*reinterpret_cast<const uint4*>(nout + (size_t)gr * DN + cb + u * 8), xv);
+#pragma unroll
+                for (int j = 0; j < 8; ++j) {
+                    float val = cex[row * 264 + cb + u * 8 + j] + xv[j] + IO<B>::ld(bn, cb + u * 8 + j);
+                    v[u * 8 + j] = val; sum += val; sq += val * val;
+                }
+            }
+            sum += __shfl_xor(sum, 1, 64); sq += __shfl_xor(sq, 1, 64);
+            sum += __shfl_xor(sum, 2, 64); sq += __shfl_xor(sq, 2, 64);
+            sum += __shfl_xor(sum, 4, 64); sq += __shfl_xor(sq, 4, 64);
+            float mu = sum * (1.f / DN);
+            float rstd = rsqrtf(fmaxf(sq * (1.f / DN) - mu * mu, 0.f) + LN_EPS);
+#pragma unroll
+            for (int u = 0; u < 4; ++u)
+#pragma unroll
+                for (int j = 0; j < 8; ++j) {
+                    int c = cb + u * 8 + j;
+                    IO<B>::st(out_nodes, (size_t)gr * DN + c,
+                              (v[u * 8 + j] - mu) * rstd * IO<B>::ld(g, c) + IO<B>::ld(b, c));
+                }
         }
     }
 }
@@ -793,96 +855,6 @@
     esum[(size_t)node * DE + lane] = a0;
     esum[(size_t)node * DE + 64 + lane] = a1;
     if (lane == 0) ecnt[node] = (float)(b1 - b0);
-}
-
-template<int B>
-__global__ __launch_bounds__(256) void k_bridge_node(
-    const int* dflag, const u16* __restrict__ nout,
-    const float* __restrict__ esum, const float* __restrict__ ecnt,
-    const void* __restrict__ Wn, const void* __restrict__ bn,
-    const void* __restrict__ g, const void* __restrict__ b, void* __restrict__ out_nodes)
-{
-    if (*dflag != B) return;
-    __shared__ __align__(16) float As[32][36];
-    __shared__ __align__(16) float Ws[32][264];
-    __shared__ float rc[32];
-    const int t = threadIdx.x;
-    const int m0 = blockIdx.x * 32;
-    if (t < 32) {
-        int gr = m0 + t;
-        rc[t] = (gr < NN) ? 1.f / (ecnt[gr] + 1e-10f) : 0.f;
-    }
-    __syncthreads();
-    const int r0 = (t >> 5) * 4;
-    const int c0 = (t & 31) * 8;
-    const int arow = t >> 3, akk = (t & 7) * 4;
-    const int wrow = t >> 3, wcc = (t & 7) * 32;
-    float acc[4][8] = {};
-    for (int k0 = 0; k0 < 384; k0 += 32) {
-        float av[4];
-        const int gr = m0 + arow;
-        if (gr < NN) {
-            if (k0 < 256) {
-                uint2 v = *reinterpret_cast<const uint2*>(nout + (size_t)gr * DN + k0 + akk);
-                av[0] = bf2f(v.x & 0xffffu); av[1] = bf2f(v.x >> 16);
-                av[2] = bf2f(v.y & 0xffffu); av[3] = bf2f(v.y >> 16);
-            } else {
-                float4 v = *reinterpret_cast<const float4*>(esum + (size_t)gr * DE + (k0 - 256) + akk);
-                float r = rc[arow];
-                av[0] = v.x * r; av[1] = v.y * r; av[2] = v.z * r; av[3] = v.w * r;
-            }
-        } else { av[0] = av[1] = av[2] = av[3] = 0.f; }
-        float wv[32];
-#pragma unroll
-        for (int u = 0; u < 4; ++u)
-            IO<B>::ld8(Wn, (size_t)(k0 + wrow) * DN + wcc + u * 8, wv + u * 8);
-        __syncthreads();
-#pragma unroll
-        for (int j = 0; j < 4; ++j) As[akk + j][arow] = av[j];
-#pragma unroll
-        for (int j = 0; j < 32; ++j) Ws[wrow][wcc + j] = wv[j];
-        __syncthreads();
-#pragma unroll
-        for (int kk = 0; kk < 32; ++kk) {
-            float4 a4 = *reinterpret_cast<const float4*>(&As[kk][r0]);
-            float4 wa = *reinterpret_cast<const float4*>(&Ws[kk][c0]);
-            float4 wb = *reinterpret_cast<const float4*>(&Ws[kk][c0 + 4]);
-            float aa[4] = {a4.x, a4.y, a4.z, a4.w};
-            float ww[8] = {wa.x, wa.y, wa.z, wa.w, wb.x, wb.y, wb.z, wb.w};
-#pragma unroll
-            for (int i = 0; i < 4; ++i)
-#pragma unroll
-                for (int j = 0; j < 8; ++j) acc[i][j] += aa[i] * ww[j];
-        }
-        __syncthreads();
-    }
-    float gv[8], bv[8], bnv[8];
-#pragma unroll
-    for (int j = 0; j < 8; ++j) {
-        gv[j] = IO<B>::ld(g, c0 + j); bv[j] = IO<B>::ld(b, c0 + j); bnv[j] = IO<B>::ld(bn, c0 + j);
-    }
-#pragma unroll
-    for (int i = 0; i < 4; ++i) {
-        int gr = m0 + r0 + i;
-        if (gr >= NN) continue;
-        float val[8]; float sum = 0.f, sq = 0.f;
-#pragma unroll
-        for (int j = 0; j < 8; ++j) {
-            val[j] = acc[i][j] + bf2f(nout[(size_t)gr * DN + c0 + j]) + bnv[j];
-            sum += val[j]; sq += val[j] * val[j];
-        }
-#pragma unroll
-        for (int msk = 1; msk < 32; msk <<= 1) {
-            sum += __shfl_xor(sum, msk, 64);
-            sq += __shfl_xor(sq, msk, 64);
-        }
-        float mu = sum * (1.f / DN);
-        float var = fmaxf(sq * (1.f / DN) - mu * mu, 0.f);
-        float rstd = rsqrtf(var + LN_EPS);
-#pragma unroll
-        for (int j = 0; j < 8; ++j)
-            IO<B>::st(out_nodes, (size_t)gr * DN + c0 + j, (val[j] - mu) * rstd * gv[j] + bv[j]);
-    }
 }
 
 extern "C" void kernel_launch(void* const* d_in, const int* in_sizes, int n_in,
@@ -934,10 +906,13 @@
     u16* WtQn = (u16*)take((size_t)DN * DN * 2);
     u16* WtKn = (u16*)take((size_t)DN * DN * 2);
     u16* WtVn = (u16*)take((size_t)DN * DN * 2);
+    u16* WtOn = (u16*)take((size_t)DN * DN * 2);
     u16* WtQe = (u16*)take((size_t)DE * DE * 2);
     u16* WtKe = (u16*)take((size_t)DE * DE * 2);
     u16* WtVe = (u16*)take((size_t)DE * DE * 2);
+    u16* WtOe = (u16*)take((size_t)DE * DE * 2);
     u16* WtWe = (u16*)take((size_t)640 * DE * 2);
+    u16* WtWn = (u16*)take((size_t)384 * DN * 2);
     const size_t T = off;
     u16*   Qn   = (u16*)(ws + T);
     u16*   Kn   = Qn + (size_t)NN * DN;
@@ -973,22 +948,25 @@
     k_detect<<<1, 64, 0, stream>>>(ng, flag);
 
     auto T2D = [&](const void* W, u16* Wt, int K, int Nd) {
-        k_transpose<<<dim3((unsigned)((K * Nd + 255) / 256)), 256, 0, stream>>>(flag, (const u16*)W, Wt, K, Nd);
-    };
-    T2D(nWq, WtQn, DN, DN); T2D(nWk, WtKn, DN, DN); T2D(nWv, WtVn, DN, DN);
-    T2D(eWq, WtQe, DE, DE); T2D(eWk, WtKe, DE, DE); T2D(eWv, WtVe, DE, DE);
-    T2D(rWe, WtWe, 640, DE);
+        dim3 gg((unsigned)((K * Nd + 255) / 256));
+        k_transpose_cvt<1><<<gg, 256, 0, stream>>>(flag, W, Wt, K, Nd);
+        k_transpose_cvt<0><<<gg, 256, 0, stream>>>(flag, W, Wt, K, Nd);
+    };
+    T2D(nWq, WtQn, DN, DN); T2D(nWk, WtKn, DN, DN); T2D(nWv, WtVn, DN, DN); T2D(nWo, WtOn, DN, DN);
+    T2D(eWq, WtQe, DE, DE); T2D(eWk, WtKe, DE, DE); T2D(eWv, WtVe, DE, DE); T2D(eWo, WtOe, DE, DE);
+    T2D(rWe, WtWe, 640, DE); T2D(rWn, WtWn, 384, DN);
+
+    auto GEMM = [&](const void* A, const u16* Wt, const void* bias, u16* out, int M, int K, int Nd) {
+        dim3 gg((unsigned)((M + 63) / 64), (unsigned)(Nd / 128));
+        k_gemm_mfma<1><<<gg, 256, 0, stream>>>(flag, A, Wt, bias, out, M, K, Nd);
+        k_gemm_mfma<0><<<gg, 256, 0, stream>>>(flag, A, Wt, bias, out, M, K, Nd);
+    };
 
     fill(denA, (long)NN * H, 0.f);
     fill(aggA, (long)NN * DN, 0.f);
-    dim3 gA((NN + 63) / 64, DN / 64);
-    dim3 gAm((NN + 63) / 64, DN / 128);
-    k_gemm_mfma<<<gAm, 256, 0, stream>>>(flag, (const u16*)nf, WtQn, (const u16*)nbq, Qn, NN, DN, DN);
-    k_gemm_bias<0><<<gA, 256, 0, stream>>>(flag, nf, nWq, nbq, Qn, NN, DN, DN);
-    k_gemm_mfma<<<gAm, 256, 0, stream>>>(flag, (const u16*)nf, WtKn, (const u16*)nbk, Kn, NN, DN, DN);
-    k_gemm_bias<0><<<gA, 256, 0, stream>>>(flag, nf, nWk, nbk, Kn, NN, DN, DN);
-    k_gemm_mfma<<<gAm, 256, 0, stream>>>(flag, (const u16*)nf, WtVn, (const u16*)nbv, Vn, NN, DN, DN);
-    k_gemm_bias<0><<<gA, 256, 0, stream>>>(flag, nf, nWv, nbv, Vn, NN, DN, DN);
+    GEMM(nf, WtQn, nbq, Qn, NN, DN, DN);
+    GEMM(nf, WtKn, nbk, Kn, NN, DN, DN);
+    GEMM(nf, WtVn, nbv, Vn, NN, DN, DN);
     const int gEH = (NE * H + 255) / 256;
     k_edge_bias<1><<<gEH, 256, 0, stream>>>(flag, ef, nWeb, nbeb, sA);
     k_edge_bias<0><<<gEH, 256, 0, stream>>>(flag, ef, nWeb, nbeb, sA);
@@ -998,47 +976,53 @@
         long n = (long)NE * DN;
         k_node_agg<<<dim3((unsigned)((n + 255) / 256)), 256, 0, stream>>>(Vn, srcN, tgtN, sA, denA, aggA);
     }
-    k_node_out<1><<<(NN + 31) / 32, 256, 0, stream>>>(flag, aggA, nf, nWo, nbo, ng, nb, node_out);
-    k_node_out<0><<<(NN + 31) / 32, 256, 0, stream>>>(flag, aggA, nf, nWo, nbo, ng, nb, node_out);
-
-    dim3 gB(NE / 64, DE / 64);
-    dim3 gBm(NE / 64, DE / 128);
-    k_gemm_mfma<<<gBm, 256, 0, stream>>>(flag, (const u16*)ef, WtQe, (const u16*)ebq, Qe, NE, DE, DE);
-    k_gemm_bias<0><<<gB, 256, 0, stream>>>(flag, ef, eWq, ebq, Qe, NE, DE, DE);
-    k_gemm_mfma<<<gBm, 256, 0, stream>>>(flag, (const u16*)ef, WtKe, (const u16*)ebk, Ke, NE, DE, DE);
-    k_gemm_bias<0><<<gB, 256, 0, stream>>>(flag, ef, eWk, ebk, Ke, NE, DE, DE);
+    {
+        dim3 gg((unsigned)((NN + 31) / 32));
+        k_node_out_mfma<1><<<gg, 256, 0, stream>>>(flag, aggA, nf, WtOn, nbo, ng, nb, node_out);
+        k_node_out_mfma<0><<<gg, 256, 0, stream>>>(flag, aggA, nf, WtOn, nbo, ng, nb, node_out);
+    }
+
+    GEMM(ef, WtQe, ebq, Qe, NE, DE, DE);
+    GEMM(ef, WtKe, ebk, Ke, NE, DE, DE);
     k_ctx_bias<1><<<gEH, 256, 0, stream>>>(flag, nf, srcN, tgtN, eWctx, ebctx, ebias);
     k_ctx_bias<0><<<gEH, 256, 0, stream>>>(flag, nf, srcN, tgtN, eWctx, ebctx, ebias);
     fill(den2, (long)NE * H, 0.f);
     const int gAH = (NA * H + 255) / 256;
     k_edge_score<1><<<gAH, 256, 0, stream>>>(flag, Qe, Ke, seA, teA, elogt, ebias, s2, den2);
     k_edge_score<0><<<gAH, 256, 0, stream>>>(flag, Qe, Ke, seA, teA, elogt, ebias, s2, den2);
-    k_gemm_mfma<<<gBm, 256, 0, stream>>>(flag, (const u16*)ef, WtVe, (const u16*)ebv, Qe , NE, DE, DE);
-    k_gemm_bias<0><<<gB, 256, 0, stream>>>(flag, ef, eWv, ebv, Qe , NE, DE, DE);
+    GEMM(ef, WtVe, ebv, Qe , NE, DE, DE);
     fill(agg2, (long)NE * DE, 0.f);
     {
         long n = (long)NA * DE;
         k_edge_agg<<<dim3((unsigned)((n + 255) / 256)), 256, 0, stream>>>(Qe , seA, teA, s2, den2, agg2);
     }
-    k_edge_out<1><<<NE / 64, 256, 0, stream>>>(flag, agg2, ef, eWo, ebo, eg, ebb, edge_out);
-    k_edge_out<0><<<NE / 64, 256, 0, stream>>>(flag, agg2, ef, eWo, ebo, eg, ebb, edge_out);
+    {
+        dim3 gg((unsigned)(NE / 64));
+        k_edge_out_mfma<1><<<gg, 256, 0, stream>>>(flag, agg2, ef, WtOe, ebo, eg, ebb, edge_out);
+        k_edge_out_mfma<0><<<gg, 256, 0, stream>>>(flag, agg2, ef, WtOe, ebo, eg, ebb, edge_out);
+    }
 
     void* out_nodes = d_out;
     void* out_edges_bf = (void*)((u16*)d_out + (size_t)NN * DN);
     void* out_edges_f  = (void*)((float*)d_out + (size_t)NN * DN);
-    k_bridge_edge_mfma<<<NE / 64, 256, 0, stream>>>(flag, edge_out, node_out, srcN, tgtN,
-                                                    WtWe, (const u16*)rbe, (const u16*)reg_, (const u16*)rebt,
-                                                    (u16*)out_edges_bf);
-    k_bridge_edge<0><<<NE / 64, 256, 0, stream>>>(flag, edge_out, node_out, srcN, tgtN,
-                                                  rWe, rbe, reg_, rebt, out_edges_f);
+    {
+        dim3 gg((unsigned)(NE / 64));
+        k_bridge_edge_mfma<1><<<gg, 256, 0, stream>>>(flag, edge_out, node_out, srcN, tgtN,
+                                                      WtWe, rbe, reg_, rebt, out_edges_bf);
+        k_bridge_edge_mfma<0><<<gg, 256, 0, stream>>>(flag, edge_out, node_out, srcN, tgtN,
+                                                      WtWe, rbe, reg_, rebt, out_edges_f);
+    }
     fill((float*)c_cur, NN, 0.f);
     k_deg<<<(NE + 255) / 256, 256, 0, stream>>>(srcN, tgtN, c_cur);
     k_scan<<<1, 256, 0, stream>>>(c_cur , c_off, c_cur , NN);
     k_place<<<(NE + 255) / 256, 256, 0, stream>>>(srcN, tgtN, c_cur, c_ent);
     k_esum_gather<1><<<(NN + 3) / 4, 256, 0, stream>>>(flag, out_edges_bf, c_off, c_ent, esum, ecnt);
     k_esum_gather<0><<<(NN + 3) / 4, 256, 0, stream>>>(flag, out_edges_f, c_off, c_ent, esum, ecnt);
-    k_bridge_node<1><<<(NN + 31) / 32, 256, 0, stream>>>(flag, node_out, esum, ecnt,
-                                                         rWn, rbn, rng, rnbt, out_nodes);
-    k_bridge_node<0><<<(NN + 31) / 32, 256, 0, stream>>>(flag, node_out, esum, ecnt,
-                                                         rWn, rbn, rng, rnbt, out_nodes);
-}
+    {
+        dim3 gg((unsigned)((NN + 31) / 32));
+        k_bridge_node_mfma<1><<<gg, 256, 0, stream>>>(flag, node_out, esum, ecnt,
+                                                      WtWn, rbn, rng, rnbt, out_nodes);
+        k_bridge_node_mfma<0><<<gg, 256, 0, stream>>>(flag, node_out, esum, ecnt,
+                                                      WtWn, rbn, rng, rnbt, out_nodes);
+    }
+}
```

New measurement: 3.387 ms. 10.1% less time.
